# Performance work log

Hardware: AMD Instinct MI355X
Metric: run time of the kernel (lower is better)

Reference implementation:

```python
import jax, jax.numpy as jnp
import numpy as np

B, DH, P, V, NP, K = 8, 1024, 64, 50257, 256, 8
SKEW = P * (P - 1) // 2


def setup_inputs() -> dict:
    key = jax.random.key(0)
    ks = jax.random.split(key, 24)
    f = jax.random.normal
    h_t = f(ks[0], (B, DH), jnp.float32)
    R = f(ks[1], (B, P, P), jnp.float32)
    A_t = 0.05 * (R - jnp.swapaxes(R, -1, -2))  # skew-symmetric
    B_t = f(ks[2], (B, NP, P), jnp.float32)
    E = f(ks[3], (V, P), jnp.float32)
    e_mask = f(ks[4], (B, P), jnp.float32)
    M = f(ks[5], (B, P, P), jnp.float32)
    G_tilde = jnp.eye(P) + 0.01 * jnp.einsum('bij,bkj->bik', M, M)  # SPD metric
    z0 = f(ks[6], (B, P), jnp.float32)
    s = lambda k_, sh: f(k_, sh, jnp.float32) * 0.02
    params = dict(
        WQ_w=s(ks[7], (DH, P)), WQ_b=jnp.zeros((P,)),
        WK_w=s(ks[8], (P, P)), WK_b=jnp.zeros((P,)),
        WV_w=s(ks[9], (P, P)), WV_b=jnp.zeros((P,)),
        WC_w=s(ks[10], (P, P)), WC_b=jnp.zeros((P,)),
        WO_w=s(ks[11], (DH, V)),
        WG_w=s(ks[12], (P, P)), WG_b=jnp.zeros((P,)),
        wgamma_w=s(ks[13], (DH + P + SKEW, 1)), wgamma_b=jnp.zeros((1,)),
        wmu_w=s(ks[14], (DH + P + 2, 1)), wmu_b=jnp.zeros((1,)),
        gdown_w=s(ks[15], (SKEW, P)),
        Sigma_inv=jnp.ones((P,)) * 0.1,
        hlie_w=s(ks[16], (DH, P)), hlie_b=jnp.zeros((P,)),
    )
    return dict(h_t=h_t, A_t=A_t, B_t=B_t, E=E, e_mask=e_mask,
                G_tilde=G_tilde, z0=z0, **params)


def _sq_riem(x, Y, G):
    # x: (B,p), Y: (B,n,p), G: (B,p,p) -> (B,n)
    d = Y - x[:, None, :]
    return jnp.einsum('bnp,bpq,bnq->bn', d, G, d)


def reference(h_t, A_t, B_t, E, e_mask, G_tilde, z0,
              WQ_w, WQ_b, WK_w, WK_b, WV_w, WV_b, WC_w, WC_b, WO_w,
              WG_w, WG_b, wgamma_w, wgamma_b, wmu_w, wmu_b,
              gdown_w, Sigma_inv, hlie_w, hlie_b):
    p = A_t.shape[-1]
    scale = 1.0 / jnp.sqrt(jnp.asarray(p, h_t.dtype))
    I = jnp.eye(p, dtype=A_t.dtype)
    Q_t = jnp.linalg.solve(I - A_t, jnp.broadcast_to(I + A_t, A_t.shape))  # Cayley map (B,p,p)
    q_t = h_t @ WQ_w + WQ_b                      # (B,p)
    B_rot = jnp.einsum('bnp,bpq->bnq', B_t, Q_t)  # (B,n,p)
    K_t = B_rot @ WK_w + WK_b
    V_t = B_rot @ WV_w + WV_b
    h_lie = h_t @ hlie_w + hlie_b                 # (B,p)
    omega = -0.5 * _sq_riem(h_lie, B_rot, G_tilde)  # (B,n)
    scores = jnp.einsum('bp,bnp->bn', q_t, K_t) * scale + omega
    alpha = jax.nn.softmax(scores, axis=-1)
    c_t = jnp.einsum('bn,bnp->bp', alpha, V_t)
    iu0, iu1 = jnp.triu_indices(p, k=1)
    g_t = A_t[:, iu0, iu1]                        # (B, skew_dim)
    E_gen = E @ WG_w + WG_b                       # (V,p)
    g_proj = g_t @ gdown_w                        # (B,p)
    diff = E_gen[None, :, :] - g_proj[:, None, :]  # (B,V,p)
    kappa = -jnp.sum(diff * diff * Sigma_inv, axis=-1)  # (B,V)
    base_logits = h_t @ WO_w                      # (B,V)
    c_rot = jnp.einsum('bp,bpq->bq', c_t @ WC_w + WC_b, Q_t)
    group_logits = c_rot @ E.T * scale + kappa
    gamma = jax.nn.sigmoid(jnp.concatenate([h_t, c_t, g_t], -1) @ wgamma_w + wgamma_b)
    logits = base_logits + gamma * group_logits
    pi = jax.nn.softmax(logits, axis=-1)
    topv, topi = jax.lax.top_k(pi, K)
    topp = topv / jnp.sum(topv, -1, keepdims=True)
    E_g = E[topi]                                 # (B,k,p) gather
    E_G = jnp.einsum('bkp,bpq->bkq', E_g, Q_t)
    E_exp = jnp.einsum('bk,bkp->bp', topp, E_G)
    H = -jnp.sum(pi * jnp.log(pi + 1e-12), -1, keepdims=True)
    rho = _sq_riem(h_lie, E_exp[:, None, :], G_tilde)  # (B,1)
    mu = jax.nn.sigmoid(jnp.concatenate([h_t, c_t, H, rho], -1) @ wmu_w + wmu_b)
    m_next = mu * e_mask + (1.0 - mu) * E_exp
    outer = m_next[:, :, None] * e_mask[:, None, :]
    A_next = A_t + 0.1 * (outer - jnp.swapaxes(outer, 1, 2))
    return logits, m_next, A_next
```

## Files before the change

kernel.cpp:

```cpp
#include <hip/hip_runtime.h>
#include <math.h>

#define NV    50257
#define OUT_M 402056
#define OUT_A 402568
#define SCALE 0.125f

#define WS_Q      0
#define WS_HTR    32768
#define WS_S      40960
#define WS_TV     45056
#define WS_C0     45120
#define WS_HLIE   47144
#define WS_W1     47656
#define WS_GH     48176
#define WS_WMAT   48192
#define WS_SC     80960
#define WS_WB     83008
#define WS_CONSTB 83520
#define WS_GAMMA  83528
#define WS_CT     83536
#define WS_P6     84048
#define WS_PQT    86016
#define WS_PHL    94208
#define WS_PGH    102400
#define WS_PGP    102528
#define WS_PGG    118912

__global__ __launch_bounds__(256) void kA_prep(
    const float* __restrict__ h_t, const float* __restrict__ A_t,
    const float* __restrict__ WG_w, const float* __restrict__ WG_b,
    const float* __restrict__ Sigma_inv,
    const float* __restrict__ WQ_w, const float* __restrict__ wgamma_w,
    const float* __restrict__ hlie_w, const float* __restrict__ gdown_w,
    float* __restrict__ ws)
{
    __shared__ float Ash[64][65];
    __shared__ float Gsh[64][65];
    __shared__ float hsh[1024];
    __shared__ float piv[2][132];
    __shared__ float fr[2][64];
    __shared__ float dsh[64];

    const int tid = threadIdx.x;
    const int blk = blockIdx.x;

    if (blk < 8) {
        const int b  = blk;
        const int i  = tid & 63;
        const int cb = __builtin_amdgcn_readfirstlane(tid >> 6);

        for (int idx = tid; idx < 4096; idx += 256)
            Ash[idx >> 6][idx & 63] = A_t[b*4096 + idx];
        for (int k = tid; k < 1024; k += 256)
            ws[WS_HTR + k*8 + b] = h_t[b*1024 + k];
        __syncthreads();

        float w[32];
        if (cb < 2) {
            #pragma unroll
            for (int jj = 0; jj < 32; ++jj) {
                int j = cb*32 + jj;
                w[jj] = (i == j ? 1.0f : 0.0f) - Ash[i][j];
            }
        } else {
            #pragma unroll
            for (int jj = 0; jj < 32; ++jj) {
                int j = (cb - 2)*32 + jj;
                w[jj] = (i == j ? 1.0f : 0.0f) + Ash[i][j];
            }
        }
        __syncthreads();

        #pragma unroll
        for (int k = 0; k < 64; ++k) {
            const int kb  = k >> 5;
            const int sel = k & 1;
            if (cb == kb) fr[sel][i] = w[k & 31];
            if (i == k) {
                #pragma unroll
                for (int q4 = 0; q4 < 8; ++q4)
                    *(float4*)&piv[sel][cb*32 + q4*4] =
                        make_float4(w[q4*4], w[q4*4+1], w[q4*4+2], w[q4*4+3]);
            }
            __syncthreads();
            float pk = piv[sel][k];
            float f = (i == k) ? 0.0f : (fr[sel][i] / pk);
            #pragma unroll
            for (int jj = 0; jj < 32; ++jj)
                w[jj] -= f * piv[sel][cb*32 + jj];
        }

        if (cb == (i >> 5)) dsh[i] = w[i & 31];
        __syncthreads();
        if (cb >= 2) {
            float dinv = 1.0f / dsh[i];
            #pragma unroll
            for (int jj = 0; jj < 32; ++jj)
                Ash[i][(cb - 2)*32 + jj] = w[jj] * dinv;
        }
        __syncthreads();
        for (int idx = tid; idx < 4096; idx += 256)
            ws[WS_Q + b*4096 + idx] = Ash[idx >> 6][idx & 63];
        return;
    }

    if (blk == 8) {
        const int a   = tid & 63;
        const int cb8 = __builtin_amdgcn_readfirstlane(tid >> 6);
        float* sig = hsh;
        float* bg  = hsh + 64;
        if (tid < 64) { sig[tid] = Sigma_inv[tid]; bg[tid] = WG_b[tid]; }
        __syncthreads();
        for (int idx = tid; idx < 4096; idx += 256) {
            int r = idx >> 6, c = idx & 63;
            float wv = WG_w[idx];
            Gsh[r][c] = wv;
            Ash[r][c] = wv * sig[c];
        }
        __syncthreads();
        float t8[16];
        #pragma unroll
        for (int j = 0; j < 16; ++j) t8[j] = 0.0f;
        for (int p = 0; p < 64; ++p) {
            float wv = Ash[a][p];
            #pragma unroll
            for (int jj = 0; jj < 16; ++jj) t8[jj] = fmaf(wv, Gsh[cb8*16 + jj][p], t8[jj]);
        }
        #pragma unroll
        for (int jj = 0; jj < 16; ++jj)
            ws[WS_S + a*64 + cb8*16 + jj] = t8[jj];
        if (cb8 == 0) {
            float s = 0.0f;
            for (int p = 0; p < 64; ++p) s += Ash[a][p] * bg[p];
            ws[WS_TV + a] = 2.0f * s;
        }
        if (tid == 0) {
            float c0 = 0.0f;
            for (int p = 0; p < 64; ++p) c0 += sig[p] * bg[p] * bg[p];
            ws[WS_C0] = c0;
        }
        return;
    }

    if (blk < 25) {
        const int c = blk - 9;
        const int i = tid & 63;
        const int w = __builtin_amdgcn_readfirstlane(tid >> 6);
        for (int idx = tid; idx < 4096; idx += 256) {
            int r = idx >> 6, col = idx & 63;
            int krow = c*64 + r;
            Ash[r][col] = WQ_w[krow*64 + col];
            Gsh[r][col] = hlie_w[krow*64 + col];
        }
        for (int t = tid; t < 512; t += 256) {
            int b = t >> 6, kk = t & 63;
            hsh[b*64 + kk] = h_t[b*1024 + c*64 + kk];
        }
        if (tid < 64) dsh[tid] = wgamma_w[c*64 + tid];
        __syncthreads();
        const int b0 = 2*w, b1 = 2*w + 1;
        float q0 = 0, q1 = 0, l0 = 0, l1 = 0;
        #pragma unroll 8
        for (int kk = 0; kk < 64; ++kk) {
            float a = Ash[kk][i], g = Gsh[kk][i];
            float h0 = hsh[b0*64 + kk], h1 = hsh[b1*64 + kk];
            q0 = fmaf(h0, a, q0); q1 = fmaf(h1, a, q1);
            l0 = fmaf(h0, g, l0); l1 = fmaf(h1, g, l1);
        }
        ws[WS_PQT + (c*8 + b0)*64 + i] = q0;
        ws[WS_PQT + (c*8 + b1)*64 + i] = q1;
        ws[WS_PHL + (c*8 + b0)*64 + i] = l0;
        ws[WS_PHL + (c*8 + b1)*64 + i] = l1;
        float g0 = hsh[b0*64 + i] * dsh[i];
        float g1 = hsh[b1*64 + i] * dsh[i];
        #pragma unroll
        for (int off = 32; off > 0; off >>= 1) {
            g0 += __shfl_xor(g0, off);
            g1 += __shfl_xor(g1, off);
        }
        if (i == 0) {
            ws[WS_PGH + c*8 + b0] = g0;
            ws[WS_PGH + c*8 + b1] = g1;
        }
        return;
    }

    {
        const int c = blk - 25;
        const int i = tid & 63;
        const int w = __builtin_amdgcn_readfirstlane(tid >> 6);
        for (int idx = tid; idx < 4032; idx += 256) {
            int r = idx >> 6, col = idx & 63;
            Ash[r][col] = gdown_w[(c*63 + r)*64 + col];
        }
        for (int t = tid; t < 504; t += 256) {
            int b = t / 63, sl = t % 63;
            int s = c*63 + sl;
            int i2 = 0, f = 0;
            while (f + (63 - i2) <= s) { f += 63 - i2; ++i2; }
            int j2 = i2 + 1 + (s - f);
            hsh[b*63 + sl] = A_t[b*4096 + i2*64 + j2];
        }
        if (tid < 63) dsh[tid] = wgamma_w[1088 + c*63 + tid];
        __syncthreads();
        const int b0 = 2*w, b1 = 2*w + 1;
        float a0 = 0, a1 = 0;
        #pragma unroll 4
        for (int sl = 0; sl < 63; ++sl) {
            float gd = Ash[sl][i];
            a0 = fmaf(hsh[b0*63 + sl], gd, a0);
            a1 = fmaf(hsh[b1*63 + sl], gd, a1);
        }
        ws[WS_PGP + (c*8 + b0)*64 + i] = a0;
        ws[WS_PGP + (c*8 + b1)*64 + i] = a1;
        float g0 = (i < 63) ? hsh[b0*63 + i] * dsh[i] : 0.0f;
        float g1 = (i < 63) ? hsh[b1*63 + i] * dsh[i] : 0.0f;
        #pragma unroll
        for (int off = 32; off > 0; off >>= 1) {
            g0 += __shfl_xor(g0, off);
            g1 += __shfl_xor(g1, off);
        }
        if (i == 0) {
            ws[WS_PGG + c*8 + b0] = g0;
            ws[WS_PGG + c*8 + b1] = g1;
        }
    }
}

__global__ __launch_bounds__(256) void kB_chain(
    const float* __restrict__ G_t,
    const float* __restrict__ WQ_b, const float* __restrict__ WK_w,
    const float* __restrict__ hlie_b,
    float* __restrict__ ws)
{
    __shared__ float Qsh[64][65], Gsh[64][65];
    __shared__ float part[4][64], partb[4][64];
    __shared__ float qt[64], hl[64], qkv[64], v0[64];
    __shared__ float red16[16];

    const int b = blockIdx.x, tid = threadIdx.x;
    const int i = tid & 63;
    const int cb = __builtin_amdgcn_readfirstlane(tid >> 6);
    const int col0 = cb * 16;

    for (int idx = tid; idx < 4096; idx += 256) {
        int r = idx >> 6, c = idx & 63;
        Qsh[r][c] = ws[WS_Q + b*4096 + idx];
        Gsh[r][c] = G_t[b*4096 + idx];
    }
    {
        float aq = 0, ah = 0;
        #pragma unroll
        for (int cc = 0; cc < 4; ++cc) {
            int c = cb*4 + cc;
            aq += ws[WS_PQT + (c*8 + b)*64 + i];
            ah += ws[WS_PHL + (c*8 + b)*64 + i];
        }
        part[cb][i] = aq; partb[cb][i] = ah;
    }
    if (tid < 16) red16[tid] = ws[WS_PGH + tid*8 + b];
    __syncthreads();
    if (tid < 64) {
        qt[tid] = part[0][tid]+part[1][tid]+part[2][tid]+part[3][tid] + WQ_b[tid];
        hl[tid] = partb[0][tid]+partb[1][tid]+partb[2][tid]+partb[3][tid] + hlie_b[tid];
    }
    if (tid == 0) {
        float s = 0;
        #pragma unroll
        for (int j = 0; j < 16; ++j) s += red16[j];
        ws[WS_GH + b] = s;
    }
    __syncthreads();
    {
        float acc = 0;
        #pragma unroll
        for (int jj = 0; jj < 16; ++jj)
            acc = fmaf(WK_w[i*64 + col0 + jj], qt[col0 + jj], acc);
        part[cb][i] = acc;
    }
    __syncthreads();
    if (tid < 64) qkv[tid] = part[0][tid]+part[1][tid]+part[2][tid]+part[3][tid];
    __syncthreads();
    {
        float acc = 0;
        #pragma unroll
        for (int jj = 0; jj < 16; ++jj)
            acc = fmaf(Gsh[i][col0 + jj], hl[col0 + jj], acc);
        part[cb][i] = acc;
    }
    __syncthreads();
    if (tid < 64)
        v0[tid] = SCALE*qkv[tid] + part[0][tid]+part[1][tid]+part[2][tid]+part[3][tid];
    __syncthreads();
    {
        float acc = 0;
        #pragma unroll
        for (int jj = 0; jj < 16; ++jj)
            acc = fmaf(Qsh[i][col0 + jj], v0[col0 + jj], acc);
        part[cb][i] = acc;
    }
    __syncthreads();
    if (tid < 64) {
        ws[WS_W1 + b*64 + tid]   = part[0][tid]+part[1][tid]+part[2][tid]+part[3][tid];
        ws[WS_HLIE + b*64 + tid] = hl[tid];
    }
    float tt[16];
    #pragma unroll
    for (int j = 0; j < 16; ++j) tt[j] = 0;
    for (int r = 0; r < 64; ++r) {
        float qv = Qsh[i][r];
        #pragma unroll
        for (int j = 0; j < 16; ++j) tt[j] = fmaf(qv, Gsh[r][col0 + j], tt[j]);
    }
    __syncthreads();
    #pragma unroll
    for (int j = 0; j < 16; ++j) Gsh[i][col0 + j] = tt[j];
    __syncthreads();
    float w2r[16];
    #pragma unroll
    for (int j = 0; j < 16; ++j) w2r[j] = 0;
    for (int q = 0; q < 64; ++q) {
        float tv = Gsh[i][q];
        #pragma unroll
        for (int j = 0; j < 16; ++j) w2r[j] = fmaf(tv, Qsh[col0 + j][q], w2r[j]);
    }
    #pragma unroll
    for (int j = 0; j < 16; ++j)
        ws[WS_WMAT + b*4096 + (col0 + j)*64 + i] = w2r[j];
}

__global__ __launch_bounds__(256) void kC_scores(
    const float* __restrict__ B_t, float* __restrict__ ws)
{
    __shared__ float Bsh[64][65];
    __shared__ float Wsh[64][64];
    __shared__ float w1sh[64];
    __shared__ float part[4][64];
    const int b = blockIdx.x >> 2, q4 = blockIdx.x & 3;
    const int tid = threadIdx.x, lane = tid & 63;
    const int gu = __builtin_amdgcn_readfirstlane(tid >> 6);
    const int col0 = gu * 16;
    for (int idx = tid; idx < 4096; idx += 256) {
        int r = idx >> 6, c = idx & 63;
        Bsh[r][c] = B_t[b*16384 + (q4*64 + r)*64 + c];
        Wsh[r][c] = ws[WS_WMAT + b*4096 + idx];
    }
    if (tid < 64) w1sh[tid] = ws[WS_W1 + b*64 + tid];
    __syncthreads();
    float t[16];
    #pragma unroll
    for (int j = 0; j < 16; ++j) t[j] = 0;
    for (int p = 0; p < 64; ++p) {
        float bv = Bsh[lane][p];
        #pragma unroll
        for (int j = 0; j < 16; ++j) t[j] = fmaf(bv, Wsh[p][col0 + j], t[j]);
    }
    float ps = 0;
    #pragma unroll
    for (int j = 0; j < 16; ++j) ps += (w1sh[col0+j] - 0.5f*t[j]) * Bsh[lane][col0+j];
    part[gu][lane] = ps;
    __syncthreads();
    if (tid < 64)
        ws[WS_SC + b*256 + q4*64 + tid] =
            part[0][tid]+part[1][tid]+part[2][tid]+part[3][tid];
}

__global__ __launch_bounds__(256) void kD_mid(
    const float* __restrict__ B_t,
    const float* __restrict__ WV_w, const float* __restrict__ WV_b,
    const float* __restrict__ WC_w, const float* __restrict__ WC_b,
    const float* __restrict__ WG_w, const float* __restrict__ WG_b,
    const float* __restrict__ wgamma_w, const float* __restrict__ wgamma_b,
    const float* __restrict__ Sigma_inv,
    float* __restrict__ ws)
{
    __shared__ float alpha[256], rr[256];
    __shared__ float part[4][64];
    __shared__ float cBr[64], cB[64], ct[64], cw[64], crot[64], gp[64], uv[64];
    __shared__ float red32[32];
    const int b = blockIdx.x, tid = threadIdx.x, lane = tid & 63;
    const int gu = __builtin_amdgcn_readfirstlane(tid >> 6);
    const int col0 = gu * 16;
    const float* Qb = ws + WS_Q + b*4096;

    float sv = ws[WS_SC + b*256 + tid];
    rr[tid] = sv;
    if (tid < 32) red32[tid] = ws[WS_PGG + tid*8 + b];
    __syncthreads();
    for (int off = 128; off > 0; off >>= 1) { if (tid < off) rr[tid] = fmaxf(rr[tid], rr[tid+off]); __syncthreads(); }
    float smax = rr[0]; __syncthreads();
    float e = expf(sv - smax);
    rr[tid] = e; __syncthreads();
    for (int off = 128; off > 0; off >>= 1) { if (tid < off) rr[tid] += rr[tid+off]; __syncthreads(); }
    float den = rr[0]; __syncthreads();
    alpha[tid] = e / den;
    __syncthreads();
    {
        float acc = 0;
        for (int nn = 0; nn < 64; ++nn) {
            int n = gu*64 + nn;
            acc = fmaf(alpha[n], B_t[b*16384 + n*64 + lane], acc);
        }
        part[gu][lane] = acc;
    }
    __syncthreads();
    if (tid < 64) cBr[tid] = part[0][tid]+part[1][tid]+part[2][tid]+part[3][tid];
    __syncthreads();
    {
        float acc = 0;
        #pragma unroll
        for (int pp = 0; pp < 16; ++pp) { int p = col0+pp; acc = fmaf(cBr[p], Qb[p*64+lane], acc); }
        part[gu][lane] = acc;
    }
    __syncthreads();
    if (tid < 64) cB[tid] = part[0][tid]+part[1][tid]+part[2][tid]+part[3][tid];
    __syncthreads();
    {
        float acc = 0;
        #pragma unroll
        for (int pp = 0; pp < 16; ++pp) { int p = col0+pp; acc = fmaf(cB[p], WV_w[p*64+lane], acc); }
        part[gu][lane] = acc;
    }
    __syncthreads();
    if (tid < 64) {
        float v = part[0][tid]+part[1][tid]+part[2][tid]+part[3][tid] + WV_b[tid];
        ct[tid] = v; ws[WS_CT + b*64 + tid] = v;
    }
    __syncthreads();
    {
        float acc = 0;
        #pragma unroll
        for (int pp = 0; pp < 16; ++pp) { int p = col0+pp; acc = fmaf(ct[p], WC_w[p*64+lane], acc); }
        part[gu][lane] = acc;
    }
    __syncthreads();
    if (tid < 64) cw[tid] = part[0][tid]+part[1][tid]+part[2][tid]+part[3][tid] + WC_b[tid];
    __syncthreads();
    {
        float acc = 0;
        #pragma unroll
        for (int pp = 0; pp < 16; ++pp) { int p = col0+pp; acc = fmaf(cw[p], Qb[p*64+lane], acc); }
        part[gu][lane] = acc;
    }
    __syncthreads();
    if (tid < 64) crot[tid] = part[0][tid]+part[1][tid]+part[2][tid]+part[3][tid];
    __syncthreads();
    {
        float acc = 0;
        #pragma unroll
        for (int cc = 0; cc < 8; ++cc) {
            int c = gu*8 + cc;
            acc += ws[WS_PGP + (c*8 + b)*64 + lane];
        }
        part[gu][lane] = acc;
    }
    if (tid < 64) rr[64 + tid] = ct[tid] * wgamma_w[1024 + tid];
    __syncthreads();
    if (tid < 64) {
        float g = part[0][tid]+part[1][tid]+part[2][tid]+part[3][tid];
        gp[tid] = g; uv[tid] = 2.0f * Sigma_inv[tid] * g;
    }
    if (tid == 0) {
        float gc = 0;
        for (int j = 0; j < 64; ++j) gc += rr[64 + j];
        float ga = 0;
        for (int j = 0; j < 32; ++j) ga += red32[j];
        float z = ws[WS_GH + b] + gc + ga + wgamma_b[0];
        ws[WS_GAMMA + b] = 1.0f / (1.0f + expf(-z));
    }
    __syncthreads();
    {
        float acc = 0;
        #pragma unroll
        for (int pp = 0; pp < 16; ++pp) { int p = col0+pp; acc = fmaf(WG_w[lane*64+p], uv[p], acc); }
        part[gu][lane] = acc;
    }
    if (tid < 64) rr[tid] = WG_b[tid]*uv[tid] - gp[tid]*gp[tid]*Sigma_inv[tid];
    __syncthreads();
    if (tid < 64)
        ws[WS_WB + b*64 + tid] = SCALE*crot[tid]
            + part[0][tid]+part[1][tid]+part[2][tid]+part[3][tid];
    if (tid == 0) { float s = 0; for (int j = 0; j < 64; ++j) s += rr[j]; ws[WS_CONSTB + b] = s; }
}

#define KU 16
__global__ __launch_bounds__(256) void k5_logits(
    const float* __restrict__ E, const float* __restrict__ WO_w,
    const float* __restrict__ ws, float* __restrict__ out)
{
    __shared__ float smem[11600];
    const int tid = threadIdx.x;
    const int q   = tid >> 6;
    const int vt  = tid & 63;
    const int vb  = blockIdx.x * 64;
    const int v   = vb + vt;
    const bool vok = v < NV;
    const int vv = vok ? v : NV - 1;

    float* Esh  = smem;
    float* Ssh  = smem + 4224;
    float* tvsh = smem + 8448;
    float* wbsh = smem + 8512;
    float* gmsh = smem + 9024;
    float* cbsh = smem + 9032;
    float* svsh = smem + 9040;
    float* gdsh = smem + 9296;
    float* accsh= smem + 9872;
    float* hsh  = smem;

    for (int idx = tid; idx < 1024; idx += 256) {
        int r = idx >> 4, c4 = (idx & 15) * 4;
        int vr = vb + r; if (vr >= NV) vr = NV - 1;
        float4 e4 = *(const float4*)(E + (size_t)vr * 64 + c4);
        float* dst = Esh + r*66 + c4;
        dst[0] = e4.x; dst[1] = e4.y; dst[2] = e4.z; dst[3] = e4.w;
    }
    for (int idx = tid; idx < 4096; idx += 256) Ssh[idx] = ws[WS_S + idx];
    for (int idx = tid; idx < 512; idx += 256) wbsh[idx] = ws[WS_WB + idx];
    if (tid < 64) tvsh[tid] = ws[WS_TV + tid];
    if (tid < 8) { gmsh[tid] = ws[WS_GAMMA + tid]; cbsh[tid] = ws[WS_CONSTB + tid]; }
    __syncthreads();
    {
        const float* er = Esh + vt*66;
        float sv = (q == 0) ? ws[WS_C0] : 0.0f;
        {
            float t[16];
            #pragma unroll
            for (int j = 0; j < 16; ++j) t[j] = 0.0f;
            for (int p = 0; p < 64; ++p) {
                float ep = er[p];
                #pragma unroll
                for (int j = 0; j < 16; ++j)
                    t[j] = fmaf(ep, Ssh[p*64 + q*16 + j], t[j]);
            }
            #pragma unroll
            for (int j = 0; j < 16; ++j)
                sv += (t[j] + tvsh[q*16 + j]) * er[q*16 + j];
        }
        svsh[q*64 + vt] = sv;
        const float* w0 = wbsh + (2*q    )*64;
        const float* w1 = wbsh + (2*q + 1)*64;
        float g0 = 0, g1 = 0;
        #pragma unroll 8
        for (int p = 0; p < 64; ++p) {
            float ep = er[p];
            g0 = fmaf(ep, w0[p], g0); g1 = fmaf(ep, w1[p], g1);
        }
        gdsh[vt*9 + 2*q]     = g0;
        gdsh[vt*9 + 2*q + 1] = g1;
    }
    __syncthreads();
    for (int idx = tid; idx < 2048; idx += 256)
        *(float4*)(hsh + idx*4) = *(const float4*)(ws + WS_HTR + idx*4);
    __syncthreads();
    float acc[8];
    #pragma unroll
    for (int bb = 0; bb < 8; ++bb) acc[bb] = 0.0f;
    {
        const float* wo = WO_w + (size_t)(q * 256) * NV + vv;
        const float* hb = hsh + q*256*8;
        for (int k0 = 0; k0 < 256; k0 += KU) {
            float wr[KU];
            #pragma unroll
            for (int u = 0; u < KU; ++u) wr[u] = wo[(size_t)(k0 + u) * NV];
            #pragma unroll
            for (int u = 0; u < KU; ++u) {
                const float* hp = hb + (k0 + u)*8;
                #pragma unroll
                for (int bb = 0; bb < 8; ++bb) acc[bb] = fmaf(hp[bb], wr[u], acc[bb]);
            }
        }
    }
    if (q) {
        float* ar = accsh + (q-1)*576 + vt*9;
        #pragma unroll
        for (int bb = 0; bb < 8; ++bb) ar[bb] = acc[bb];
    }
    __syncthreads();
    if (q == 0 && vok) {
        float svt = svsh[vt] + svsh[64+vt] + svsh[128+vt] + svsh[192+vt];
        const float* gr = gdsh + vt*9;
        #pragma unroll
        for (int bb = 0; bb < 8; ++bb) {
            float a = acc[bb] + accsh[vt*9+bb] + accsh[576+vt*9+bb] + accsh[1152+vt*9+bb];
            float gl = gr[bb] + cbsh[bb] - svt;
            out[bb*NV + v] = fmaf(gmsh[bb], gl, a);
        }
    }
}

#define NQ 12565
__global__ __launch_bounds__(256) void k6a_scan(
    const float* __restrict__ outl, float* __restrict__ ws)
{
    __shared__ float mvw[4][8];
    __shared__ int   miw[4][8];
    __shared__ float t8v[8];
    __shared__ int   t8i[8];
    __shared__ float redv[4], sred[4];
    const int b = blockIdx.x >> 2, qq = blockIdx.x & 3;
    const int tid = threadIdx.x, lane = tid & 63, wvi = tid >> 6;
    const int v0 = qq * NQ;
    const int v1 = (v0 + NQ < NV) ? (v0 + NQ) : NV;
    const float* lg = outl + b*NV;

    float lv[8]; int li[8];
    #pragma unroll
    for (int u = 0; u < 8; ++u) { lv[u] = -INFINITY; li[u] = 0x7fffffff; }
    float mt = -INFINITY, s1 = 0.0f, s2 = 0.0f;
    for (int v = v0 + tid; v < v1; v += 256) {
        float x = lg[v];
        if (x > mt) {
            float r = expf(mt - x);
            s1 *= r; s2 *= r; mt = x;
        }
        float ee = expf(x - mt);
        s1 += ee; s2 += x * ee;
        if (x > lv[7]) {
            float cv = x; int ci = v;
            #pragma unroll
            for (int u = 0; u < 8; ++u) {
                if (cv > lv[u]) {
                    float tv = lv[u]; lv[u] = cv; cv = tv;
                    int   ti = li[u]; li[u] = ci; ci = ti;
                }
            }
        }
    }
    float wv8[8]; int wi8[8];
    #pragma unroll
    for (int it = 0; it < 8; ++it) {
        float bv = lv[0]; int bi = li[0];
        #pragma unroll
        for (int off = 32; off > 0; off >>= 1) {
            float ov = __shfl_xor(bv, off);
            int   oi = __shfl_xor(bi, off);
            if (ov > bv || (ov == bv && oi < bi)) { bv = ov; bi = oi; }
        }
        wv8[it] = bv; wi8[it] = bi;
        if (lv[0] == bv && li[0] == bi) {
            lv[0]=lv[1]; lv[1]=lv[2]; lv[2]=lv[3]; lv[3]=lv[4];
            lv[4]=lv[5]; lv[5]=lv[6]; lv[6]=lv[7]; lv[7]=-INFINITY;
            li[0]=li[1]; li[1]=li[2]; li[2]=li[3]; li[3]=li[4];
            li[4]=li[5]; li[5]=li[6]; li[6]=li[7]; li[7]=0x7fffffff;
        }
    }
    if (lane == 0) {
        #pragma unroll
        for (int u = 0; u < 8; ++u) { mvw[wvi][u] = wv8[u]; miw[wvi][u] = wi8[u]; }
    }
    __syncthreads();
    if (tid == 0) {
        int pA = 0, pB = 0, pC = 0, pD = 0;
        for (int it = 0; it < 8; ++it) {
            float vA = mvw[0][pA], vB = mvw[1][pB], vC = mvw[2][pC], vD = mvw[3][pD];
            int   iA = miw[0][pA], iB = miw[1][pB], iC = miw[2][pC], iD = miw[3][pD];
            float best = vA; int bi = iA; int w = 0;
            if (vB > best || (vB == best && iB < bi)) { best = vB; bi = iB; w = 1; }
            if (vC > best || (vC == best && iC < bi)) { best = vC; bi = iC; w = 2; }
            if (vD > best || (vD == best && iD < bi)) { best = vD; bi = iD; w = 3; }
            t8v[it] = best; t8i[it] = bi;
            if (w == 0) ++pA; else if (w == 1) ++pB; else if (w == 2) ++pC; else ++pD;
        }
    }
    __syncthreads();
    float Mp = t8v[0];
    {
        float r = expf(mt - Mp);
        s1 *= r; s2 *= r;
    }
    #pragma unroll
    for (int off = 32; off > 0; off >>= 1) {
        s1 += __shfl_xor(s1, off);
        s2 += __shfl_xor(s2, off);
    }
    if (lane == 0) { redv[wvi] = s1; sred[wvi] = s2; }
    __syncthreads();
    if (tid == 0) {
        int base = WS_P6 + (b*4 + qq)*20;
        #pragma unroll
        for (int u = 0; u < 8; ++u) { ws[base + u] = t8v[u]; ((int*)ws)[base + 8 + u] = t8i[u]; }
        ws[base + 16] = Mp;
        ws[base + 17] = redv[0]+redv[1]+redv[2]+redv[3];
        ws[base + 18] = sred[0]+sred[1]+sred[2]+sred[3];
    }
}

__global__ __launch_bounds__(256) void k6b_final(
    const float* __restrict__ h_t, const float* __restrict__ A_t,
    const float* __restrict__ E, const float* __restrict__ e_mask,
    const float* __restrict__ G_t,
    const float* __restrict__ wmu_w, const float* __restrict__ wmu_b,
    const float* __restrict__ ws, float* __restrict__ out)
{
    __shared__ float mv[32];
    __shared__ int   mi[32];
    __shared__ float t8v[8];
    __shared__ int   t8i[8];
    __shared__ float toppsh[8];
    __shared__ float redv[256];
    __shared__ float uvec[64], eexp[64], msh[64], emsh[64];
    __shared__ float scal[4];
    const int b = blockIdx.x, tid = threadIdx.x;

    if (tid < 32) {
        int base = WS_P6 + (b*4 + (tid >> 3))*20;
        mv[tid] = ws[base + (tid & 7)];
        mi[tid] = ((const int*)ws)[base + 8 + (tid & 7)];
    }
    __syncthreads();
    if (tid == 0) {
        unsigned used = 0;
        for (int it = 0; it < 8; ++it) {
            float best = -INFINITY; int bi = 0x7fffffff, bs = 0;
            for (int c = 0; c < 32; ++c) {
                if (used & (1u << c)) continue;
                float x = mv[c];
                if (x > best || (x == best && mi[c] < bi)) { best = x; bi = mi[c]; bs = c; }
            }
            used |= 1u << bs; t8v[it] = best; t8i[it] = bi;
        }
        float M = t8v[0];
        float s1 = 0, s2 = 0;
        for (int q = 0; q < 4; ++q) {
            int base = WS_P6 + (b*4 + q)*20;
            float sc_ = expf(ws[base + 16] - M);
            s1 += ws[base + 17] * sc_; s2 += ws[base + 18] * sc_;
        }
        scal[0] = M + logf(s1) - s2 / s1;
        float ts = 0, tv_[8];
        #pragma unroll
        for (int u = 0; u < 8; ++u) { tv_[u] = expf(t8v[u] - M); ts += tv_[u]; }
        #pragma unroll
        for (int u = 0; u < 8; ++u) toppsh[u] = tv_[u] / ts;
    }
    __syncthreads();
    if (tid < 64) {
        float u_ = 0;
        #pragma unroll
        for (int j = 0; j < 8; ++j) u_ += toppsh[j] * E[t8i[j]*64 + tid];
        uvec[tid] = u_;
    }
    __syncthreads();
    if (tid < 64) {
        const float* Qb = ws + WS_Q + b*4096;
        float a = 0;
        for (int p = 0; p < 64; ++p) a += uvec[p] * Qb[p*64 + tid];
        eexp[tid] = a;
    }
    __syncthreads();
    {
        const float* Gb = G_t + b*4096;
        const float* HL = ws + WS_HLIE + b*64;
        float a = 0;
        #pragma unroll 4
        for (int t2 = 0; t2 < 16; ++t2) {
            int idx = tid*16 + t2;
            int p = idx >> 6, q = idx & 63;
            a += (eexp[p] - HL[p]) * Gb[idx] * (eexp[q] - HL[q]);
        }
        redv[tid] = a;
    }
    __syncthreads();
    for (int off = 128; off > 0; off >>= 1) {
        if (tid < off) redv[tid] += redv[tid + off];
        __syncthreads();
    }
    if (tid == 0) scal[1] = redv[0];
    __syncthreads();
    float pm = 0;
    for (int k = tid; k < 1024; k += 256) pm += h_t[b*1024 + k] * wmu_w[k];
    if (tid < 64) pm += ws[WS_CT + b*64 + tid] * wmu_w[1024 + tid];
    redv[tid] = pm;
    __syncthreads();
    for (int off = 128; off > 0; off >>= 1) {
        if (tid < off) redv[tid] += redv[tid + off];
        __syncthreads();
    }
    if (tid == 0) {
        float z = redv[0] + scal[0]*wmu_w[1088] + scal[1]*wmu_w[1089] + wmu_b[0];
        scal[2] = 1.0f / (1.0f + expf(-z));
    }
    __syncthreads();
    if (tid < 64) {
        float mu = scal[2];
        float em = e_mask[b*64 + tid];
        float m = mu*em + (1.0f - mu)*eexp[tid];
        out[OUT_M + b*64 + tid] = m;
        msh[tid] = m; emsh[tid] = em;
    }
    __syncthreads();
    for (int idx = tid; idx < 4096; idx += 256) {
        int i = idx >> 6, j = idx & 63;
        out[OUT_A + b*4096 + idx] = A_t[b*4096 + idx]
            + 0.1f*(msh[i]*emsh[j] - msh[j]*emsh[i]);
    }
}

extern "C" void kernel_launch(void* const* d_in, const int* in_sizes, int n_in,
                              void* d_out, int out_size, void* d_ws, size_t ws_size,
                              hipStream_t stream)
{
    const float* h_t      = (const float*)d_in[0];
    const float* A_t      = (const float*)d_in[1];
    const float* B_t      = (const float*)d_in[2];
    const float* E        = (const float*)d_in[3];
    const float* e_mask   = (const float*)d_in[4];
    const float* G_t      = (const float*)d_in[5];
    const float* WQ_w     = (const float*)d_in[7];
    const float* WQ_b     = (const float*)d_in[8];
    const float* WK_w     = (const float*)d_in[9];
    const float* WV_w     = (const float*)d_in[11];
    const float* WV_b     = (const float*)d_in[12];
    const float* WC_w     = (const float*)d_in[13];
    const float* WC_b     = (const float*)d_in[14];
    const float* WO_w     = (const float*)d_in[15];
    const float* WG_w     = (const float*)d_in[16];
    const float* WG_b     = (const float*)d_in[17];
    const float* wgamma_w = (const float*)d_in[18];
    const float* wgamma_b = (const float*)d_in[19];
    const float* wmu_w    = (const float*)d_in[20];
    const float* wmu_b    = (const float*)d_in[21];
    const float* gdown_w  = (const float*)d_in[22];
    const float* Sigma_inv= (const float*)d_in[23];
    const float* hlie_w   = (const float*)d_in[24];
    const float* hlie_b   = (const float*)d_in[25];
    float* out = (float*)d_out;
    float* ws  = (float*)d_ws;

    kA_prep<<<57, 256, 0, stream>>>(h_t, A_t, WG_w, WG_b, Sigma_inv,
                                    WQ_w, wgamma_w, hlie_w, gdown_w, ws);
    kB_chain<<<8, 256, 0, stream>>>(G_t, WQ_b, WK_w, hlie_b, ws);
    kC_scores<<<32, 256, 0, stream>>>(B_t, ws);
    kD_mid<<<8, 256, 0, stream>>>(B_t, WV_w, WV_b, WC_w, WC_b, WG_w, WG_b,
                                  wgamma_w, wgamma_b, Sigma_inv, ws);
    k5_logits<<<786, 256, 0, stream>>>(E, WO_w, ws, out);
    k6a_scan<<<32, 256, 0, stream>>>(out, ws);
    k6b_final<<<8, 256, 0, stream>>>(h_t, A_t, E, e_mask, G_t, wmu_w, wmu_b, ws, out);
}
```

Before: 524.5 us.

## Fuse pipeline stages into a persistent cooperative megakernel with grid syncs

Replaces the chain of seven separate kernel launches with one cooperative persistent kernel that runs each stage as a device function, separated by grid-wide syncs. It keeps the original multi-launch path as a fallback. The logits stage also appears to be split into two passes (k5a/k5b) with per-block persistent setup and chunk loops. The goal is to remove launch gaps and small-kernel tail effects. In exchange it adds grid-sync overhead, a grid capped by occupancy, and a larger fixed shared-memory footprint per block.

```diff
diff --git a/kernel.cpp b/kernel.cpp
--- a/kernel.cpp
+++ b/kernel.cpp
@@ -1,5 +1,8 @@
 #include <hip/hip_runtime.h>
+#include <hip/hip_cooperative_groups.h>
 #include <math.h>
+
+namespace cg = cooperative_groups;
 
 #define NV    50257
 #define OUT_M 402056
@@ -26,367 +29,377 @@
 #define WS_PGH    102400
 #define WS_PGP    102528
 #define WS_PGG    118912
-
-__global__ __launch_bounds__(256) void kA_prep(
-    const float* __restrict__ h_t, const float* __restrict__ A_t,
-    const float* __restrict__ WG_w, const float* __restrict__ WG_b,
-    const float* __restrict__ Sigma_inv,
-    const float* __restrict__ WQ_w, const float* __restrict__ wgamma_w,
-    const float* __restrict__ hlie_w, const float* __restrict__ gdown_w,
-    float* __restrict__ ws)
-{
-    __shared__ float Ash[64][65];
-    __shared__ float Gsh[64][65];
-    __shared__ float hsh[1024];
-    __shared__ float piv[2][132];
-    __shared__ float fr[2][64];
-    __shared__ float dsh[64];
-
+#define WS_GL     131072
+
+#define SM_FLOATS 9760
+
+struct P {
+    const float *h_t, *A_t, *G_t, *B_t, *E, *e_mask;
+    const float *WG_w, *WG_b, *Sigma_inv, *WQ_w, *WQ_b, *WK_w;
+    const float *WV_w, *WV_b, *WC_w, *WC_b, *WO_w;
+    const float *wgamma_w, *wgamma_b, *wmu_w, *wmu_b, *gdown_w, *hlie_w, *hlie_b;
+    float *ws, *out;
+};
+
+
+__device__ void d_gj(float* sm, const P& p, int b)
+{
     const int tid = threadIdx.x;
-    const int blk = blockIdx.x;
-
-    if (blk < 8) {
-        const int b  = blk;
-        const int i  = tid & 63;
-        const int cb = __builtin_amdgcn_readfirstlane(tid >> 6);
-
-        for (int idx = tid; idx < 4096; idx += 256)
-            Ash[idx >> 6][idx & 63] = A_t[b*4096 + idx];
-        for (int k = tid; k < 1024; k += 256)
-            ws[WS_HTR + k*8 + b] = h_t[b*1024 + k];
+    const int i  = tid & 63;
+    const int cb = __builtin_amdgcn_readfirstlane(tid >> 6);
+    float* A   = sm;
+    float* piv = sm + 4160;
+    float* fr  = sm + 4424;
+    float* dsh = sm + 4552;
+    for (int idx = tid; idx < 4096; idx += 256)
+        A[(idx >> 6)*65 + (idx & 63)] = p.A_t[b*4096 + idx];
+    for (int k = tid; k < 1024; k += 256)
+        p.ws[WS_HTR + k*8 + b] = p.h_t[b*1024 + k];
+    __syncthreads();
+    float w[32];
+    if (cb < 2) {
+        #pragma unroll
+        for (int jj = 0; jj < 32; ++jj) {
+            int j = cb*32 + jj;
+            w[jj] = (i == j ? 1.0f : 0.0f) - A[i*65 + j];
+        }
+    } else {
+        #pragma unroll
+        for (int jj = 0; jj < 32; ++jj) {
+            int j = (cb - 2)*32 + jj;
+            w[jj] = (i == j ? 1.0f : 0.0f) + A[i*65 + j];
+        }
+    }
+    __syncthreads();
+    #pragma unroll
+    for (int k = 0; k < 64; ++k) {
+        const int kb = k >> 5, sel = k & 1;
+        if (cb == kb) fr[sel*64 + i] = w[k & 31];
+        if (i == k) {
+            #pragma unroll
+            for (int q4 = 0; q4 < 8; ++q4)
+                *(float4*)&piv[sel*132 + cb*32 + q4*4] =
+                    make_float4(w[q4*4], w[q4*4+1], w[q4*4+2], w[q4*4+3]);
+        }
         __syncthreads();
-
-        float w[32];
-        if (cb < 2) {
-            #pragma unroll
-            for (int jj = 0; jj < 32; ++jj) {
-                int j = cb*32 + jj;
-                w[jj] = (i == j ? 1.0f : 0.0f) - Ash[i][j];
-            }
-        } else {
-            #pragma unroll
-            for (int jj = 0; jj < 32; ++jj) {
-                int j = (cb - 2)*32 + jj;
-                w[jj] = (i == j ? 1.0f : 0.0f) + Ash[i][j];
-            }
-        }
-        __syncthreads();
-
-        #pragma unroll
-        for (int k = 0; k < 64; ++k) {
-            const int kb  = k >> 5;
-            const int sel = k & 1;
-            if (cb == kb) fr[sel][i] = w[k & 31];
-            if (i == k) {
-                #pragma unroll
-                for (int q4 = 0; q4 < 8; ++q4)
-                    *(float4*)&piv[sel][cb*32 + q4*4] =
-                        make_float4(w[q4*4], w[q4*4+1], w[q4*4+2], w[q4*4+3]);
-            }
-            __syncthreads();
-            float pk = piv[sel][k];
-            float f = (i == k) ? 0.0f : (fr[sel][i] / pk);
-            #pragma unroll
-            for (int jj = 0; jj < 32; ++jj)
-                w[jj] -= f * piv[sel][cb*32 + jj];
-        }
-
-        if (cb == (i >> 5)) dsh[i] = w[i & 31];
-        __syncthreads();
-        if (cb >= 2) {
-            float dinv = 1.0f / dsh[i];
-            #pragma unroll
-            for (int jj = 0; jj < 32; ++jj)
-                Ash[i][(cb - 2)*32 + jj] = w[jj] * dinv;
-        }
-        __syncthreads();
-        for (int idx = tid; idx < 4096; idx += 256)
-            ws[WS_Q + b*4096 + idx] = Ash[idx >> 6][idx & 63];
-        return;
-    }
-
-    if (blk == 8) {
-        const int a   = tid & 63;
-        const int cb8 = __builtin_amdgcn_readfirstlane(tid >> 6);
-        float* sig = hsh;
-        float* bg  = hsh + 64;
-        if (tid < 64) { sig[tid] = Sigma_inv[tid]; bg[tid] = WG_b[tid]; }
-        __syncthreads();
-        for (int idx = tid; idx < 4096; idx += 256) {
-            int r = idx >> 6, c = idx & 63;
-            float wv = WG_w[idx];
-            Gsh[r][c] = wv;
-            Ash[r][c] = wv * sig[c];
-        }
-        __syncthreads();
-        float t8[16];
-        #pragma unroll
-        for (int j = 0; j < 16; ++j) t8[j] = 0.0f;
-        for (int p = 0; p < 64; ++p) {
-            float wv = Ash[a][p];
-            #pragma unroll
-            for (int jj = 0; jj < 16; ++jj) t8[jj] = fmaf(wv, Gsh[cb8*16 + jj][p], t8[jj]);
-        }
+        float pk = piv[sel*132 + k];
+        float f = (i == k) ? 0.0f : (fr[sel*64 + i] / pk);
+        #pragma unroll
+        for (int jj = 0; jj < 32; ++jj)
+            w[jj] -= f * piv[sel*132 + cb*32 + jj];
+    }
+    if (cb == (i >> 5)) dsh[i] = w[i & 31];
+    __syncthreads();
+    if (cb >= 2) {
+        float dinv = 1.0f / dsh[i];
+        #pragma unroll
+        for (int jj = 0; jj < 32; ++jj)
+            A[i*65 + (cb - 2)*32 + jj] = w[jj] * dinv;
+    }
+    __syncthreads();
+    for (int idx = tid; idx < 4096; idx += 256)
+        p.ws[WS_Q + b*4096 + idx] = A[(idx >> 6)*65 + (idx & 63)];
+    __syncthreads();
+}
+
+__device__ void d_sphase(float* sm, const P& p)
+{
+    const int tid = threadIdx.x;
+    const int a   = tid & 63;
+    const int cb8 = __builtin_amdgcn_readfirstlane(tid >> 6);
+    float* sig = sm;
+    float* bg  = sm + 64;
+    float* Wsc = sm + 128;
+    float* Wr  = sm + 4288;
+    if (tid < 64) { sig[tid] = p.Sigma_inv[tid]; bg[tid] = p.WG_b[tid]; }
+    __syncthreads();
+    for (int idx = tid; idx < 4096; idx += 256) {
+        int r = idx >> 6, c = idx & 63;
+        float wv = p.WG_w[idx];
+        Wr[r*65 + c]  = wv;
+        Wsc[r*65 + c] = wv * sig[c];
+    }
+    __syncthreads();
+    float t8[16];
+    #pragma unroll
+    for (int j = 0; j < 16; ++j) t8[j] = 0.0f;
+    for (int pp = 0; pp < 64; ++pp) {
+        float wv = Wsc[a*65 + pp];
         #pragma unroll
         for (int jj = 0; jj < 16; ++jj)
-            ws[WS_S + a*64 + cb8*16 + jj] = t8[jj];
-        if (cb8 == 0) {
-            float s = 0.0f;
-            for (int p = 0; p < 64; ++p) s += Ash[a][p] * bg[p];
-            ws[WS_TV + a] = 2.0f * s;
-        }
-        if (tid == 0) {
-            float c0 = 0.0f;
-            for (int p = 0; p < 64; ++p) c0 += sig[p] * bg[p] * bg[p];
-            ws[WS_C0] = c0;
-        }
-        return;
-    }
-
-    if (blk < 25) {
-        const int c = blk - 9;
-        const int i = tid & 63;
-        const int w = __builtin_amdgcn_readfirstlane(tid >> 6);
-        for (int idx = tid; idx < 4096; idx += 256) {
-            int r = idx >> 6, col = idx & 63;
-            int krow = c*64 + r;
-            Ash[r][col] = WQ_w[krow*64 + col];
-            Gsh[r][col] = hlie_w[krow*64 + col];
-        }
-        for (int t = tid; t < 512; t += 256) {
-            int b = t >> 6, kk = t & 63;
-            hsh[b*64 + kk] = h_t[b*1024 + c*64 + kk];
-        }
-        if (tid < 64) dsh[tid] = wgamma_w[c*64 + tid];
-        __syncthreads();
-        const int b0 = 2*w, b1 = 2*w + 1;
-        float q0 = 0, q1 = 0, l0 = 0, l1 = 0;
-        #pragma unroll 8
-        for (int kk = 0; kk < 64; ++kk) {
-            float a = Ash[kk][i], g = Gsh[kk][i];
-            float h0 = hsh[b0*64 + kk], h1 = hsh[b1*64 + kk];
-            q0 = fmaf(h0, a, q0); q1 = fmaf(h1, a, q1);
-            l0 = fmaf(h0, g, l0); l1 = fmaf(h1, g, l1);
-        }
-        ws[WS_PQT + (c*8 + b0)*64 + i] = q0;
-        ws[WS_PQT + (c*8 + b1)*64 + i] = q1;
-        ws[WS_PHL + (c*8 + b0)*64 + i] = l0;
-        ws[WS_PHL + (c*8 + b1)*64 + i] = l1;
-        float g0 = hsh[b0*64 + i] * dsh[i];
-        float g1 = hsh[b1*64 + i] * dsh[i];
-        #pragma unroll
-        for (int off = 32; off > 0; off >>= 1) {
-            g0 += __shfl_xor(g0, off);
-            g1 += __shfl_xor(g1, off);
-        }
-        if (i == 0) {
-            ws[WS_PGH + c*8 + b0] = g0;
-            ws[WS_PGH + c*8 + b1] = g1;
-        }
-        return;
-    }
-
-    {
-        const int c = blk - 25;
-        const int i = tid & 63;
-        const int w = __builtin_amdgcn_readfirstlane(tid >> 6);
-        for (int idx = tid; idx < 4032; idx += 256) {
-            int r = idx >> 6, col = idx & 63;
-            Ash[r][col] = gdown_w[(c*63 + r)*64 + col];
-        }
-        for (int t = tid; t < 504; t += 256) {
-            int b = t / 63, sl = t % 63;
-            int s = c*63 + sl;
-            int i2 = 0, f = 0;
-            while (f + (63 - i2) <= s) { f += 63 - i2; ++i2; }
-            int j2 = i2 + 1 + (s - f);
-            hsh[b*63 + sl] = A_t[b*4096 + i2*64 + j2];
-        }
-        if (tid < 63) dsh[tid] = wgamma_w[1088 + c*63 + tid];
-        __syncthreads();
-        const int b0 = 2*w, b1 = 2*w + 1;
-        float a0 = 0, a1 = 0;
-        #pragma unroll 4
-        for (int sl = 0; sl < 63; ++sl) {
-            float gd = Ash[sl][i];
-            a0 = fmaf(hsh[b0*63 + sl], gd, a0);
-            a1 = fmaf(hsh[b1*63 + sl], gd, a1);
-        }
-        ws[WS_PGP + (c*8 + b0)*64 + i] = a0;
-        ws[WS_PGP + (c*8 + b1)*64 + i] = a1;
-        float g0 = (i < 63) ? hsh[b0*63 + i] * dsh[i] : 0.0f;
-        float g1 = (i < 63) ? hsh[b1*63 + i] * dsh[i] : 0.0f;
-        #pragma unroll
-        for (int off = 32; off > 0; off >>= 1) {
-            g0 += __shfl_xor(g0, off);
-            g1 += __shfl_xor(g1, off);
-        }
-        if (i == 0) {
-            ws[WS_PGG + c*8 + b0] = g0;
-            ws[WS_PGG + c*8 + b1] = g1;
-        }
-    }
-}
-
-__global__ __launch_bounds__(256) void kB_chain(
-    const float* __restrict__ G_t,
-    const float* __restrict__ WQ_b, const float* __restrict__ WK_w,
-    const float* __restrict__ hlie_b,
-    float* __restrict__ ws)
-{
-    __shared__ float Qsh[64][65], Gsh[64][65];
-    __shared__ float part[4][64], partb[4][64];
-    __shared__ float qt[64], hl[64], qkv[64], v0[64];
-    __shared__ float red16[16];
-
-    const int b = blockIdx.x, tid = threadIdx.x;
+            t8[jj] = fmaf(wv, Wr[(cb8*16 + jj)*65 + pp], t8[jj]);
+    }
+    #pragma unroll
+    for (int jj = 0; jj < 16; ++jj)
+        p.ws[WS_S + a*64 + cb8*16 + jj] = t8[jj];
+    if (cb8 == 0) {
+        float s = 0.0f;
+        for (int pp = 0; pp < 64; ++pp) s += Wsc[a*65 + pp] * bg[pp];
+        p.ws[WS_TV + a] = 2.0f * s;
+    }
+    if (tid == 0) {
+        float c0 = 0.0f;
+        for (int pp = 0; pp < 64; ++pp) c0 += sig[pp] * bg[pp] * bg[pp];
+        p.ws[WS_C0] = c0;
+    }
+    __syncthreads();
+}
+
+__device__ void d_hgemv(float* sm, const P& p, int c)
+{
+    const int tid = threadIdx.x;
+    const int i = tid & 63;
+    const int w = __builtin_amdgcn_readfirstlane(tid >> 6);
+    float* WQs = sm;
+    float* HLs = sm + 4160;
+    float* hh  = sm + 8320;
+    float* dd  = sm + 8832;
+    for (int idx = tid; idx < 4096; idx += 256) {
+        int r = idx >> 6, col = idx & 63;
+        int krow = c*64 + r;
+        WQs[r*65 + col] = p.WQ_w[krow*64 + col];
+        HLs[r*65 + col] = p.hlie_w[krow*64 + col];
+    }
+    for (int t = tid; t < 512; t += 256) {
+        int b = t >> 6, kk = t & 63;
+        hh[b*64 + kk] = p.h_t[b*1024 + c*64 + kk];
+    }
+    if (tid < 64) dd[tid] = p.wgamma_w[c*64 + tid];
+    __syncthreads();
+    const int b0 = 2*w, b1 = 2*w + 1;
+    float q0 = 0, q1 = 0, l0 = 0, l1 = 0;
+    #pragma unroll 8
+    for (int kk = 0; kk < 64; ++kk) {
+        float a = WQs[kk*65 + i], g = HLs[kk*65 + i];
+        float h0 = hh[b0*64 + kk], h1 = hh[b1*64 + kk];
+        q0 = fmaf(h0, a, q0); q1 = fmaf(h1, a, q1);
+        l0 = fmaf(h0, g, l0); l1 = fmaf(h1, g, l1);
+    }
+    p.ws[WS_PQT + (c*8 + b0)*64 + i] = q0;
+    p.ws[WS_PQT + (c*8 + b1)*64 + i] = q1;
+    p.ws[WS_PHL + (c*8 + b0)*64 + i] = l0;
+    p.ws[WS_PHL + (c*8 + b1)*64 + i] = l1;
+    float g0 = hh[b0*64 + i] * dd[i];
+    float g1 = hh[b1*64 + i] * dd[i];
+    #pragma unroll
+    for (int off = 32; off > 0; off >>= 1) {
+        g0 += __shfl_xor(g0, off);
+        g1 += __shfl_xor(g1, off);
+    }
+    if (i == 0) {
+        p.ws[WS_PGH + c*8 + b0] = g0;
+        p.ws[WS_PGH + c*8 + b1] = g1;
+    }
+    __syncthreads();
+}
+
+__device__ void d_gdown(float* sm, const P& p, int c)
+{
+    const int tid = threadIdx.x;
+    const int i = tid & 63;
+    const int w = __builtin_amdgcn_readfirstlane(tid >> 6);
+    float* GD = sm;
+    float* hh = sm + 4160;
+    float* dd = sm + 4672;
+    for (int idx = tid; idx < 4032; idx += 256) {
+        int r = idx >> 6, col = idx & 63;
+        GD[r*65 + col] = p.gdown_w[(c*63 + r)*64 + col];
+    }
+    for (int t = tid; t < 504; t += 256) {
+        int b = t / 63, sl = t % 63;
+        int s = c*63 + sl;
+        int i2 = 0, f = 0;
+        while (f + (63 - i2) <= s) { f += 63 - i2; ++i2; }
+        int j2 = i2 + 1 + (s - f);
+        hh[b*63 + sl] = p.A_t[b*4096 + i2*64 + j2];
+    }
+    if (tid < 63) dd[tid] = p.wgamma_w[1088 + c*63 + tid];
+    __syncthreads();
+    const int b0 = 2*w, b1 = 2*w + 1;
+    float a0 = 0, a1 = 0;
+    #pragma unroll 4
+    for (int sl = 0; sl < 63; ++sl) {
+        float gd = GD[sl*65 + i];
+        a0 = fmaf(hh[b0*63 + sl], gd, a0);
+        a1 = fmaf(hh[b1*63 + sl], gd, a1);
+    }
+    p.ws[WS_PGP + (c*8 + b0)*64 + i] = a0;
+    p.ws[WS_PGP + (c*8 + b1)*64 + i] = a1;
+    float g0 = (i < 63) ? hh[b0*63 + i] * dd[i] : 0.0f;
+    float g1 = (i < 63) ? hh[b1*63 + i] * dd[i] : 0.0f;
+    #pragma unroll
+    for (int off = 32; off > 0; off >>= 1) {
+        g0 += __shfl_xor(g0, off);
+        g1 += __shfl_xor(g1, off);
+    }
+    if (i == 0) {
+        p.ws[WS_PGG + c*8 + b0] = g0;
+        p.ws[WS_PGG + c*8 + b1] = g1;
+    }
+    __syncthreads();
+}
+
+__device__ void d_kB(float* sm, const P& p, int b)
+{
+    const int tid = threadIdx.x;
     const int i = tid & 63;
     const int cb = __builtin_amdgcn_readfirstlane(tid >> 6);
     const int col0 = cb * 16;
+    float* Q     = sm;
+    float* G     = sm + 4160;
+    float* part  = sm + 8320;
+    float* partb = sm + 8576;
+    float* qt    = sm + 8832;
+    float* hl    = sm + 8896;
+    float* qkv   = sm + 8960;
+    float* v0    = sm + 9024;
+    float* r16   = sm + 9088;
 
     for (int idx = tid; idx < 4096; idx += 256) {
         int r = idx >> 6, c = idx & 63;
-        Qsh[r][c] = ws[WS_Q + b*4096 + idx];
-        Gsh[r][c] = G_t[b*4096 + idx];
+        Q[r*65 + c] = p.ws[WS_Q + b*4096 + idx];
+        G[r*65 + c] = p.G_t[b*4096 + idx];
     }
     {
         float aq = 0, ah = 0;
         #pragma unroll
         for (int cc = 0; cc < 4; ++cc) {
             int c = cb*4 + cc;
-            aq += ws[WS_PQT + (c*8 + b)*64 + i];
-            ah += ws[WS_PHL + (c*8 + b)*64 + i];
-        }
-        part[cb][i] = aq; partb[cb][i] = ah;
-    }
-    if (tid < 16) red16[tid] = ws[WS_PGH + tid*8 + b];
+            aq += p.ws[WS_PQT + (c*8 + b)*64 + i];
+            ah += p.ws[WS_PHL + (c*8 + b)*64 + i];
+        }
+        part[cb*64 + i] = aq; partb[cb*64 + i] = ah;
+    }
+    if (tid < 16) r16[tid] = p.ws[WS_PGH + tid*8 + b];
     __syncthreads();
     if (tid < 64) {
-        qt[tid] = part[0][tid]+part[1][tid]+part[2][tid]+part[3][tid] + WQ_b[tid];
-        hl[tid] = partb[0][tid]+partb[1][tid]+partb[2][tid]+partb[3][tid] + hlie_b[tid];
+        qt[tid] = part[tid]+part[64+tid]+part[128+tid]+part[192+tid] + p.WQ_b[tid];
+        hl[tid] = partb[tid]+partb[64+tid]+partb[128+tid]+partb[192+tid] + p.hlie_b[tid];
     }
     if (tid == 0) {
         float s = 0;
         #pragma unroll
-        for (int j = 0; j < 16; ++j) s += red16[j];
-        ws[WS_GH + b] = s;
+        for (int j = 0; j < 16; ++j) s += r16[j];
+        p.ws[WS_GH + b] = s;
     }
     __syncthreads();
     {
         float acc = 0;
         #pragma unroll
         for (int jj = 0; jj < 16; ++jj)
-            acc = fmaf(WK_w[i*64 + col0 + jj], qt[col0 + jj], acc);
-        part[cb][i] = acc;
-    }
-    __syncthreads();
-    if (tid < 64) qkv[tid] = part[0][tid]+part[1][tid]+part[2][tid]+part[3][tid];
+            acc = fmaf(p.WK_w[i*64 + col0 + jj], qt[col0 + jj], acc);
+        part[cb*64 + i] = acc;
+    }
+    __syncthreads();
+    if (tid < 64) qkv[tid] = part[tid]+part[64+tid]+part[128+tid]+part[192+tid];
     __syncthreads();
     {
         float acc = 0;
         #pragma unroll
         for (int jj = 0; jj < 16; ++jj)
-            acc = fmaf(Gsh[i][col0 + jj], hl[col0 + jj], acc);
-        part[cb][i] = acc;
+            acc = fmaf(G[i*65 + col0 + jj], hl[col0 + jj], acc);
+        part[cb*64 + i] = acc;
     }
     __syncthreads();
     if (tid < 64)
-        v0[tid] = SCALE*qkv[tid] + part[0][tid]+part[1][tid]+part[2][tid]+part[3][tid];
+        v0[tid] = SCALE*qkv[tid] + part[tid]+part[64+tid]+part[128+tid]+part[192+tid];
     __syncthreads();
     {
         float acc = 0;
         #pragma unroll
         for (int jj = 0; jj < 16; ++jj)
-            acc = fmaf(Qsh[i][col0 + jj], v0[col0 + jj], acc);
-        part[cb][i] = acc;
+            acc = fmaf(Q[i*65 + col0 + jj], v0[col0 + jj], acc);
+        part[cb*64 + i] = acc;
     }
     __syncthreads();
     if (tid < 64) {
-        ws[WS_W1 + b*64 + tid]   = part[0][tid]+part[1][tid]+part[2][tid]+part[3][tid];
-        ws[WS_HLIE + b*64 + tid] = hl[tid];
+        p.ws[WS_W1 + b*64 + tid]   = part[tid]+part[64+tid]+part[128+tid]+part[192+tid];
+        p.ws[WS_HLIE + b*64 + tid] = hl[tid];
     }
     float tt[16];
     #pragma unroll
     for (int j = 0; j < 16; ++j) tt[j] = 0;
     for (int r = 0; r < 64; ++r) {
-        float qv = Qsh[i][r];
-        #pragma unroll
-        for (int j = 0; j < 16; ++j) tt[j] = fmaf(qv, Gsh[r][col0 + j], tt[j]);
-    }
-    __syncthreads();
-    #pragma unroll
-    for (int j = 0; j < 16; ++j) Gsh[i][col0 + j] = tt[j];
+        float qv = Q[i*65 + r];
+        #pragma unroll
+        for (int j = 0; j < 16; ++j) tt[j] = fmaf(qv, G[r*65 + col0 + j], tt[j]);
+    }
+    __syncthreads();
+    #pragma unroll
+    for (int j = 0; j < 16; ++j) G[i*65 + col0 + j] = tt[j];
     __syncthreads();
     float w2r[16];
     #pragma unroll
     for (int j = 0; j < 16; ++j) w2r[j] = 0;
     for (int q = 0; q < 64; ++q) {
-        float tv = Gsh[i][q];
-        #pragma unroll
-        for (int j = 0; j < 16; ++j) w2r[j] = fmaf(tv, Qsh[col0 + j][q], w2r[j]);
+        float tv = G[i*65 + q];
+        #pragma unroll
+        for (int j = 0; j < 16; ++j) w2r[j] = fmaf(tv, Q[(col0 + j)*65 + q], w2r[j]);
     }
     #pragma unroll
     for (int j = 0; j < 16; ++j)
-        ws[WS_WMAT + b*4096 + (col0 + j)*64 + i] = w2r[j];
-}
-
-__global__ __launch_bounds__(256) void kC_scores(
-    const float* __restrict__ B_t, float* __restrict__ ws)
-{
-    __shared__ float Bsh[64][65];
-    __shared__ float Wsh[64][64];
-    __shared__ float w1sh[64];
-    __shared__ float part[4][64];
-    const int b = blockIdx.x >> 2, q4 = blockIdx.x & 3;
+        p.ws[WS_WMAT + b*4096 + (col0 + j)*64 + i] = w2r[j];
+    __syncthreads();
+}
+
+__device__ void d_kC(float* sm, const P& p, int j)
+{
+    const int b = j >> 2, q4 = j & 3;
     const int tid = threadIdx.x, lane = tid & 63;
     const int gu = __builtin_amdgcn_readfirstlane(tid >> 6);
     const int col0 = gu * 16;
+    float* B    = sm;
+    float* W    = sm + 4160;
+    float* w1   = sm + 8256;
+    float* part = sm + 8320;
     for (int idx = tid; idx < 4096; idx += 256) {
         int r = idx >> 6, c = idx & 63;
-        Bsh[r][c] = B_t[b*16384 + (q4*64 + r)*64 + c];
-        Wsh[r][c] = ws[WS_WMAT + b*4096 + idx];
-    }
-    if (tid < 64) w1sh[tid] = ws[WS_W1 + b*64 + tid];
+        B[r*65 + c] = p.B_t[b*16384 + (q4*64 + r)*64 + c];
+        W[idx]      = p.ws[WS_WMAT + b*4096 + idx];
+    }
+    if (tid < 64) w1[tid] = p.ws[WS_W1 + b*64 + tid];
     __syncthreads();
     float t[16];
     #pragma unroll
-    for (int j = 0; j < 16; ++j) t[j] = 0;
-    for (int p = 0; p < 64; ++p) {
-        float bv = Bsh[lane][p];
-        #pragma unroll
-        for (int j = 0; j < 16; ++j) t[j] = fmaf(bv, Wsh[p][col0 + j], t[j]);
+    for (int jj = 0; jj < 16; ++jj) t[jj] = 0;
+    for (int pp = 0; pp < 64; ++pp) {
+        float bv = B[lane*65 + pp];
+        #pragma unroll
+        for (int jj = 0; jj < 16; ++jj) t[jj] = fmaf(bv, W[pp*64 + col0 + jj], t[jj]);
     }
     float ps = 0;
     #pragma unroll
-    for (int j = 0; j < 16; ++j) ps += (w1sh[col0+j] - 0.5f*t[j]) * Bsh[lane][col0+j];
-    part[gu][lane] = ps;
+    for (int jj = 0; jj < 16; ++jj)
+        ps += (w1[col0+jj] - 0.5f*t[jj]) * B[lane*65 + col0 + jj];
+    part[gu*64 + lane] = ps;
     __syncthreads();
     if (tid < 64)
-        ws[WS_SC + b*256 + q4*64 + tid] =
-            part[0][tid]+part[1][tid]+part[2][tid]+part[3][tid];
-}
-
-__global__ __launch_bounds__(256) void kD_mid(
-    const float* __restrict__ B_t,
-    const float* __restrict__ WV_w, const float* __restrict__ WV_b,
-    const float* __restrict__ WC_w, const float* __restrict__ WC_b,
-    const float* __restrict__ WG_w, const float* __restrict__ WG_b,
-    const float* __restrict__ wgamma_w, const float* __restrict__ wgamma_b,
-    const float* __restrict__ Sigma_inv,
-    float* __restrict__ ws)
-{
-    __shared__ float alpha[256], rr[256];
-    __shared__ float part[4][64];
-    __shared__ float cBr[64], cB[64], ct[64], cw[64], crot[64], gp[64], uv[64];
-    __shared__ float red32[32];
-    const int b = blockIdx.x, tid = threadIdx.x, lane = tid & 63;
+        p.ws[WS_SC + b*256 + q4*64 + tid] =
+            part[tid]+part[64+tid]+part[128+tid]+part[192+tid];
+    __syncthreads();
+}
+
+__device__ void d_kD(float* sm, const P& p, int b)
+{
+    const int tid = threadIdx.x, lane = tid & 63;
     const int gu = __builtin_amdgcn_readfirstlane(tid >> 6);
     const int col0 = gu * 16;
-    const float* Qb = ws + WS_Q + b*4096;
-
-    float sv = ws[WS_SC + b*256 + tid];
+    const float* Qb = p.ws + WS_Q + b*4096;
+    float* alpha = sm;
+    float* rr    = sm + 256;
+    float* part  = sm + 512;
+    float* cBr   = sm + 768;
+    float* cB    = sm + 832;
+    float* ct    = sm + 896;
+    float* cw    = sm + 960;
+    float* crot  = sm + 1024;
+    float* gp    = sm + 1088;
+    float* uv    = sm + 1152;
+    float* red32 = sm + 1216;
+
+    float sv = p.ws[WS_SC + b*256 + tid];
     rr[tid] = sv;
-    if (tid < 32) red32[tid] = ws[WS_PGG + tid*8 + b];
+    if (tid < 32) red32[tid] = p.ws[WS_PGG + tid*8 + b];
     __syncthreads();
     for (int off = 128; off > 0; off >>= 1) { if (tid < off) rr[tid] = fmaxf(rr[tid], rr[tid+off]); __syncthreads(); }
     float smax = rr[0]; __syncthreads();
@@ -400,210 +413,236 @@
         float acc = 0;
         for (int nn = 0; nn < 64; ++nn) {
             int n = gu*64 + nn;
-            acc = fmaf(alpha[n], B_t[b*16384 + n*64 + lane], acc);
-        }
-        part[gu][lane] = acc;
-    }
-    __syncthreads();
-    if (tid < 64) cBr[tid] = part[0][tid]+part[1][tid]+part[2][tid]+part[3][tid];
+            acc = fmaf(alpha[n], p.B_t[b*16384 + n*64 + lane], acc);
+        }
+        part[gu*64 + lane] = acc;
+    }
+    __syncthreads();
+    if (tid < 64) cBr[tid] = part[tid]+part[64+tid]+part[128+tid]+part[192+tid];
     __syncthreads();
     {
         float acc = 0;
         #pragma unroll
-        for (int pp = 0; pp < 16; ++pp) { int p = col0+pp; acc = fmaf(cBr[p], Qb[p*64+lane], acc); }
-        part[gu][lane] = acc;
-    }
-    __syncthreads();
-    if (tid < 64) cB[tid] = part[0][tid]+part[1][tid]+part[2][tid]+part[3][tid];
+        for (int pp = 0; pp < 16; ++pp) { int q = col0+pp; acc = fmaf(cBr[q], Qb[q*64+lane], acc); }
+        part[gu*64 + lane] = acc;
+    }
+    __syncthreads();
+    if (tid < 64) cB[tid] = part[tid]+part[64+tid]+part[128+tid]+part[192+tid];
     __syncthreads();
     {
         float acc = 0;
         #pragma unroll
-        for (int pp = 0; pp < 16; ++pp) { int p = col0+pp; acc = fmaf(cB[p], WV_w[p*64+lane], acc); }
-        part[gu][lane] = acc;
+        for (int pp = 0; pp < 16; ++pp) { int q = col0+pp; acc = fmaf(cB[q], p.WV_w[q*64+lane], acc); }
+        part[gu*64 + lane] = acc;
     }
     __syncthreads();
     if (tid < 64) {
-        float v = part[0][tid]+part[1][tid]+part[2][tid]+part[3][tid] + WV_b[tid];
-        ct[tid] = v; ws[WS_CT + b*64 + tid] = v;
+        float v = part[tid]+part[64+tid]+part[128+tid]+part[192+tid] + p.WV_b[tid];
+        ct[tid] = v; p.ws[WS_CT + b*64 + tid] = v;
     }
     __syncthreads();
     {
         float acc = 0;
         #pragma unroll
-        for (int pp = 0; pp < 16; ++pp) { int p = col0+pp; acc = fmaf(ct[p], WC_w[p*64+lane], acc); }
-        part[gu][lane] = acc;
-    }
-    __syncthreads();
-    if (tid < 64) cw[tid] = part[0][tid]+part[1][tid]+part[2][tid]+part[3][tid] + WC_b[tid];
+        for (int pp = 0; pp < 16; ++pp) { int q = col0+pp; acc = fmaf(ct[q], p.WC_w[q*64+lane], acc); }
+        part[gu*64 + lane] = acc;
+    }
+    __syncthreads();
+    if (tid < 64) cw[tid] = part[tid]+part[64+tid]+part[128+tid]+part[192+tid] + p.WC_b[tid];
     __syncthreads();
     {
         float acc = 0;
         #pragma unroll
-        for (int pp = 0; pp < 16; ++pp) { int p = col0+pp; acc = fmaf(cw[p], Qb[p*64+lane], acc); }
-        part[gu][lane] = acc;
-    }
-    __syncthreads();
-    if (tid < 64) crot[tid] = part[0][tid]+part[1][tid]+part[2][tid]+part[3][tid];
+        for (int pp = 0; pp < 16; ++pp) { int q = col0+pp; acc = fmaf(cw[q], Qb[q*64+lane], acc); }
+        part[gu*64 + lane] = acc;
+    }
+    __syncthreads();
+    if (tid < 64) crot[tid] = part[tid]+part[64+tid]+part[128+tid]+part[192+tid];
     __syncthreads();
     {
         float acc = 0;
         #pragma unroll
         for (int cc = 0; cc < 8; ++cc) {
             int c = gu*8 + cc;
-            acc += ws[WS_PGP + (c*8 + b)*64 + lane];
-        }
-        part[gu][lane] = acc;
-    }
-    if (tid < 64) rr[64 + tid] = ct[tid] * wgamma_w[1024 + tid];
+            acc += p.ws[WS_PGP + (c*8 + b)*64 + lane];
+        }
+        part[gu*64 + lane] = acc;
+    }
+    if (tid < 64) rr[64 + tid] = ct[tid] * p.wgamma_w[1024 + tid];
     __syncthreads();
     if (tid < 64) {
-        float g = part[0][tid]+part[1][tid]+part[2][tid]+part[3][tid];
-        gp[tid] = g; uv[tid] = 2.0f * Sigma_inv[tid] * g;
+        float g = part[tid]+part[64+tid]+part[128+tid]+part[192+tid];
+        gp[tid] = g; uv[tid] = 2.0f * p.Sigma_inv[tid] * g;
     }
     if (tid == 0) {
         float gc = 0;
         for (int j = 0; j < 64; ++j) gc += rr[64 + j];
         float ga = 0;
         for (int j = 0; j < 32; ++j) ga += red32[j];
-        float z = ws[WS_GH + b] + gc + ga + wgamma_b[0];
-        ws[WS_GAMMA + b] = 1.0f / (1.0f + expf(-z));
+        float z = p.ws[WS_GH + b] + gc + ga + p.wgamma_b[0];
+        p.ws[WS_GAMMA + b] = 1.0f / (1.0f + expf(-z));
     }
     __syncthreads();
     {
         float acc = 0;
         #pragma unroll
-        for (int pp = 0; pp < 16; ++pp) { int p = col0+pp; acc = fmaf(WG_w[lane*64+p], uv[p], acc); }
-        part[gu][lane] = acc;
-    }
-    if (tid < 64) rr[tid] = WG_b[tid]*uv[tid] - gp[tid]*gp[tid]*Sigma_inv[tid];
+        for (int pp = 0; pp < 16; ++pp) { int q = col0+pp; acc = fmaf(p.WG_w[lane*64+q], uv[q], acc); }
+        part[gu*64 + lane] = acc;
+    }
+    if (tid < 64) rr[tid] = p.WG_b[tid]*uv[tid] - gp[tid]*gp[tid]*p.Sigma_inv[tid];
     __syncthreads();
     if (tid < 64)
-        ws[WS_WB + b*64 + tid] = SCALE*crot[tid]
-            + part[0][tid]+part[1][tid]+part[2][tid]+part[3][tid];
-    if (tid == 0) { float s = 0; for (int j = 0; j < 64; ++j) s += rr[j]; ws[WS_CONSTB + b] = s; }
-}
-
-#define KU 16
-__global__ __launch_bounds__(256) void k5_logits(
-    const float* __restrict__ E, const float* __restrict__ WO_w,
-    const float* __restrict__ ws, float* __restrict__ out)
-{
-    __shared__ float smem[11600];
+        p.ws[WS_WB + b*64 + tid] = SCALE*crot[tid]
+            + part[tid]+part[64+tid]+part[128+tid]+part[192+tid];
+    if (tid == 0) { float s = 0; for (int j = 0; j < 64; ++j) s += rr[j]; p.ws[WS_CONSTB + b] = s; }
+    __syncthreads();
+}
+
+__device__ void d_k5a_persist(float* sm, const P& p)
+{
     const int tid = threadIdx.x;
-    const int q   = tid >> 6;
-    const int vt  = tid & 63;
-    const int vb  = blockIdx.x * 64;
-    const int v   = vb + vt;
+    for (int idx = tid; idx < 4096; idx += 256) sm[idx] = p.ws[WS_S + idx];
+    if (tid < 64) sm[4096 + tid] = p.ws[WS_TV + tid];
+    for (int idx = tid; idx < 512; idx += 256) sm[4160 + idx] = p.ws[WS_WB + idx];
+    if (tid < 8) {
+        sm[4672 + tid] = p.ws[WS_GAMMA + tid];
+        sm[4680 + tid] = p.ws[WS_CONSTB + tid];
+    }
+}
+
+__device__ void d_k5a_chunk(float* sm, const P& p, int c)
+{
+    const int tid = threadIdx.x;
+    const int vt = tid & 63;
+    const int q  = __builtin_amdgcn_readfirstlane(tid >> 6);
+    const int vb = c * 64;
+    const int v  = vb + vt;
     const bool vok = v < NV;
-    const int vv = vok ? v : NV - 1;
-
-    float* Esh  = smem;
-    float* Ssh  = smem + 4224;
-    float* tvsh = smem + 8448;
-    float* wbsh = smem + 8512;
-    float* gmsh = smem + 9024;
-    float* cbsh = smem + 9032;
-    float* svsh = smem + 9040;
-    float* gdsh = smem + 9296;
-    float* accsh= smem + 9872;
-    float* hsh  = smem;
+    float* S  = sm;
+    float* tv = sm + 4096;
+    float* wb = sm + 4160;
+    float* gm = sm + 4672;
+    float* cbs= sm + 4680;
+    float* E  = sm + 4688;
+    float* svs= sm + 8912;
+    float* gds= sm + 9168;
 
     for (int idx = tid; idx < 1024; idx += 256) {
         int r = idx >> 4, c4 = (idx & 15) * 4;
         int vr = vb + r; if (vr >= NV) vr = NV - 1;
-        float4 e4 = *(const float4*)(E + (size_t)vr * 64 + c4);
-        float* dst = Esh + r*66 + c4;
+        float4 e4 = *(const float4*)(p.E + (size_t)vr * 64 + c4);
+        float* dst = E + r*66 + c4;
         dst[0] = e4.x; dst[1] = e4.y; dst[2] = e4.z; dst[3] = e4.w;
     }
-    for (int idx = tid; idx < 4096; idx += 256) Ssh[idx] = ws[WS_S + idx];
-    for (int idx = tid; idx < 512; idx += 256) wbsh[idx] = ws[WS_WB + idx];
-    if (tid < 64) tvsh[tid] = ws[WS_TV + tid];
-    if (tid < 8) { gmsh[tid] = ws[WS_GAMMA + tid]; cbsh[tid] = ws[WS_CONSTB + tid]; }
-    __syncthreads();
-    {
-        const float* er = Esh + vt*66;
-        float sv = (q == 0) ? ws[WS_C0] : 0.0f;
-        {
-            float t[16];
-            #pragma unroll
-            for (int j = 0; j < 16; ++j) t[j] = 0.0f;
-            for (int p = 0; p < 64; ++p) {
-                float ep = er[p];
-                #pragma unroll
-                for (int j = 0; j < 16; ++j)
-                    t[j] = fmaf(ep, Ssh[p*64 + q*16 + j], t[j]);
-            }
+    __syncthreads();
+    {
+        const float* er = E + vt*66;
+        float sv = (q == 0) ? p.ws[WS_C0] : 0.0f;
+        float t[16];
+        #pragma unroll
+        for (int j = 0; j < 16; ++j) t[j] = 0.0f;
+        for (int pp = 0; pp < 64; ++pp) {
+            float ep = er[pp];
             #pragma unroll
             for (int j = 0; j < 16; ++j)
-                sv += (t[j] + tvsh[q*16 + j]) * er[q*16 + j];
-        }
-        svsh[q*64 + vt] = sv;
-        const float* w0 = wbsh + (2*q    )*64;
-        const float* w1 = wbsh + (2*q + 1)*64;
+                t[j] = fmaf(ep, S[pp*64 + q*16 + j], t[j]);
+        }
+        #pragma unroll
+        for (int j = 0; j < 16; ++j)
+            sv += (t[j] + tv[q*16 + j]) * er[q*16 + j];
+        svs[q*64 + vt] = sv;
+        const float* w0 = wb + (2*q    )*64;
+        const float* w1 = wb + (2*q + 1)*64;
         float g0 = 0, g1 = 0;
         #pragma unroll 8
-        for (int p = 0; p < 64; ++p) {
-            float ep = er[p];
-            g0 = fmaf(ep, w0[p], g0); g1 = fmaf(ep, w1[p], g1);
-        }
-        gdsh[vt*9 + 2*q]     = g0;
-        gdsh[vt*9 + 2*q + 1] = g1;
-    }
-    __syncthreads();
+        for (int pp = 0; pp < 64; ++pp) {
+            float ep = er[pp];
+            g0 = fmaf(ep, w0[pp], g0); g1 = fmaf(ep, w1[pp], g1);
+        }
+        gds[vt*9 + 2*q]     = g0;
+        gds[vt*9 + 2*q + 1] = g1;
+    }
+    __syncthreads();
+    if (q == 0 && vok) {
+        float svt = svs[vt] + svs[64+vt] + svs[128+vt] + svs[192+vt];
+        const float* gr = gds + vt*9;
+        #pragma unroll
+        for (int bb = 0; bb < 8; ++bb)
+            p.ws[WS_GL + bb*NV + v] = gm[bb] * (gr[bb] + cbs[bb] - svt);
+    }
+}
+
+__device__ void d_k5b_persist(float* sm, const P& p)
+{
+    const int tid = threadIdx.x;
     for (int idx = tid; idx < 2048; idx += 256)
-        *(float4*)(hsh + idx*4) = *(const float4*)(ws + WS_HTR + idx*4);
-    __syncthreads();
+        *(float4*)(sm + idx*4) = *(const float4*)(p.ws + WS_HTR + idx*4);
+}
+
+__device__ void d_k5b_chunk(float* sm, const P& p, int c)
+{
+    const int tid = threadIdx.x;
+    const int vt = tid & 63;
+    const int kg = __builtin_amdgcn_readfirstlane(tid >> 6);
+    const int vb = c * 64;
+    const int v  = vb + vt;
+    const bool vok = v < NV;
+    const int vv = vok ? v : NV - 1;
+    float* h   = sm;
+    float* red = sm + 8192;
+
     float acc[8];
     #pragma unroll
     for (int bb = 0; bb < 8; ++bb) acc[bb] = 0.0f;
     {
-        const float* wo = WO_w + (size_t)(q * 256) * NV + vv;
-        const float* hb = hsh + q*256*8;
-        for (int k0 = 0; k0 < 256; k0 += KU) {
-            float wr[KU];
+        const float* wo = p.WO_w + (size_t)(kg * 256) * NV + vv;
+        const float* hb = h + kg*256*8;
+        for (int k0 = 0; k0 < 256; k0 += 8) {
+            float wr[8];
             #pragma unroll
-            for (int u = 0; u < KU; ++u) wr[u] = wo[(size_t)(k0 + u) * NV];
+            for (int u = 0; u < 8; ++u) wr[u] = wo[(size_t)(k0 + u) * NV];
             #pragma unroll
-            for (int u = 0; u < KU; ++u) {
+            for (int u = 0; u < 8; ++u) {
                 const float* hp = hb + (k0 + u)*8;
                 #pragma unroll
                 for (int bb = 0; bb < 8; ++bb) acc[bb] = fmaf(hp[bb], wr[u], acc[bb]);
             }
         }
     }
-    if (q) {
-        float* ar = accsh + (q-1)*576 + vt*9;
-        #pragma unroll
-        for (int bb = 0; bb < 8; ++bb) ar[bb] = acc[bb];
-    }
-    __syncthreads();
-    if (q == 0 && vok) {
-        float svt = svsh[vt] + svsh[64+vt] + svsh[128+vt] + svsh[192+vt];
-        const float* gr = gdsh + vt*9;
-        #pragma unroll
-        for (int bb = 0; bb < 8; ++bb) {
-            float a = acc[bb] + accsh[vt*9+bb] + accsh[576+vt*9+bb] + accsh[1152+vt*9+bb];
-            float gl = gr[bb] + cbsh[bb] - svt;
-            out[bb*NV + v] = fmaf(gmsh[bb], gl, a);
-        }
+    float gl[8];
+    if (kg == 0) {
+        #pragma unroll
+        for (int bb = 0; bb < 8; ++bb) gl[bb] = p.ws[WS_GL + bb*NV + vv];
+    }
+    __syncthreads();
+    if (kg >= 1) {
+        float* r = red + (kg - 1)*512 + vt*8;
+        #pragma unroll
+        for (int bb = 0; bb < 8; ++bb) r[bb] = acc[bb];
+    }
+    __syncthreads();
+    if (kg == 0 && vok) {
+        #pragma unroll
+        for (int bb = 0; bb < 8; ++bb)
+            p.out[bb*NV + v] = acc[bb] + red[vt*8+bb] + red[512+vt*8+bb]
+                             + red[1024+vt*8+bb] + gl[bb];
     }
 }
 
 #define NQ 12565
-__global__ __launch_bounds__(256) void k6a_scan(
-    const float* __restrict__ outl, float* __restrict__ ws)
-{
-    __shared__ float mvw[4][8];
-    __shared__ int   miw[4][8];
-    __shared__ float t8v[8];
-    __shared__ int   t8i[8];
-    __shared__ float redv[4], sred[4];
-    const int b = blockIdx.x >> 2, qq = blockIdx.x & 3;
+__device__ void d_k6a(float* sm, const P& p, int j)
+{
+    const int b = j >> 2, qq = j & 3;
     const int tid = threadIdx.x, lane = tid & 63, wvi = tid >> 6;
     const int v0 = qq * NQ;
     const int v1 = (v0 + NQ < NV) ? (v0 + NQ) : NV;
-    const float* lg = outl + b*NV;
+    const float* lg = p.out + b*NV;
+    float* mvw = sm;
+    int*   miw = (int*)(sm + 32);
+    float* t8v = sm + 64;
+    int*   t8i = (int*)(sm + 72);
+    float* redv= sm + 80;
+    float* sred= sm + 84;
 
     float lv[8]; int li[8];
     #pragma unroll
@@ -622,7 +661,7 @@
             #pragma unroll
             for (int u = 0; u < 8; ++u) {
                 if (cv > lv[u]) {
-                    float tv = lv[u]; lv[u] = cv; cv = tv;
+                    float tv2 = lv[u]; lv[u] = cv; cv = tv2;
                     int   ti = li[u]; li[u] = ci; ci = ti;
                 }
             }
@@ -648,14 +687,14 @@
     }
     if (lane == 0) {
         #pragma unroll
-        for (int u = 0; u < 8; ++u) { mvw[wvi][u] = wv8[u]; miw[wvi][u] = wi8[u]; }
+        for (int u = 0; u < 8; ++u) { mvw[wvi*8 + u] = wv8[u]; miw[wvi*8 + u] = wi8[u]; }
     }
     __syncthreads();
     if (tid == 0) {
         int pA = 0, pB = 0, pC = 0, pD = 0;
         for (int it = 0; it < 8; ++it) {
-            float vA = mvw[0][pA], vB = mvw[1][pB], vC = mvw[2][pC], vD = mvw[3][pD];
-            int   iA = miw[0][pA], iB = miw[1][pB], iC = miw[2][pC], iD = miw[3][pD];
+            float vA = mvw[0*8+pA], vB = mvw[1*8+pB], vC = mvw[2*8+pC], vD = mvw[3*8+pD];
+            int   iA = miw[0*8+pA], iB = miw[1*8+pB], iC = miw[2*8+pC], iD = miw[3*8+pD];
             float best = vA; int bi = iA; int w = 0;
             if (vB > best || (vB == best && iB < bi)) { best = vB; bi = iB; w = 1; }
             if (vC > best || (vC == best && iC < bi)) { best = vC; bi = iC; w = 2; }
@@ -680,34 +719,33 @@
     if (tid == 0) {
         int base = WS_P6 + (b*4 + qq)*20;
         #pragma unroll
-        for (int u = 0; u < 8; ++u) { ws[base + u] = t8v[u]; ((int*)ws)[base + 8 + u] = t8i[u]; }
-        ws[base + 16] = Mp;
-        ws[base + 17] = redv[0]+redv[1]+redv[2]+redv[3];
-        ws[base + 18] = sred[0]+sred[1]+sred[2]+sred[3];
-    }
-}
-
-__global__ __launch_bounds__(256) void k6b_final(
-    const float* __restrict__ h_t, const float* __restrict__ A_t,
-    const float* __restrict__ E, const float* __restrict__ e_mask,
-    const float* __restrict__ G_t,
-    const float* __restrict__ wmu_w, const float* __restrict__ wmu_b,
-    const float* __restrict__ ws, float* __restrict__ out)
-{
-    __shared__ float mv[32];
-    __shared__ int   mi[32];
-    __shared__ float t8v[8];
-    __shared__ int   t8i[8];
-    __shared__ float toppsh[8];
-    __shared__ float redv[256];
-    __shared__ float uvec[64], eexp[64], msh[64], emsh[64];
-    __shared__ float scal[4];
-    const int b = blockIdx.x, tid = threadIdx.x;
+        for (int u = 0; u < 8; ++u) { p.ws[base + u] = t8v[u]; ((int*)p.ws)[base + 8 + u] = t8i[u]; }
+        p.ws[base + 16] = Mp;
+        p.ws[base + 17] = redv[0]+redv[1]+redv[2]+redv[3];
+        p.ws[base + 18] = sred[0]+sred[1]+sred[2]+sred[3];
+    }
+    __syncthreads();
+}
+
+__device__ void d_k6b(float* sm, const P& p, int b)
+{
+    const int tid = threadIdx.x;
+    float* mv   = sm;
+    int*   mi   = (int*)(sm + 32);
+    float* t8v  = sm + 64;
+    int*   t8i  = (int*)(sm + 72);
+    float* topp = sm + 80;
+    float* scal = sm + 88;
+    float* uvec = sm + 96;
+    float* eexp = sm + 160;
+    float* msh  = sm + 224;
+    float* emsh = sm + 288;
+    float* redv = sm + 352;
 
     if (tid < 32) {
         int base = WS_P6 + (b*4 + (tid >> 3))*20;
-        mv[tid] = ws[base + (tid & 7)];
-        mi[tid] = ((const int*)ws)[base + 8 + (tid & 7)];
+        mv[tid] = p.ws[base + (tid & 7)];
+        mi[tid] = ((const int*)p.ws)[base + 8 + (tid & 7)];
     }
     __syncthreads();
     if (tid == 0) {
@@ -725,40 +763,40 @@
         float s1 = 0, s2 = 0;
         for (int q = 0; q < 4; ++q) {
             int base = WS_P6 + (b*4 + q)*20;
-            float sc_ = expf(ws[base + 16] - M);
-            s1 += ws[base + 17] * sc_; s2 += ws[base + 18] * sc_;
+            float sc_ = expf(p.ws[base + 16] - M);
+            s1 += p.ws[base + 17] * sc_; s2 += p.ws[base + 18] * sc_;
         }
         scal[0] = M + logf(s1) - s2 / s1;
         float ts = 0, tv_[8];
         #pragma unroll
         for (int u = 0; u < 8; ++u) { tv_[u] = expf(t8v[u] - M); ts += tv_[u]; }
         #pragma unroll
-        for (int u = 0; u < 8; ++u) toppsh[u] = tv_[u] / ts;
+        for (int u = 0; u < 8; ++u) topp[u] = tv_[u] / ts;
     }
     __syncthreads();
     if (tid < 64) {
         float u_ = 0;
         #pragma unroll
-        for (int j = 0; j < 8; ++j) u_ += toppsh[j] * E[t8i[j]*64 + tid];
+        for (int j = 0; j < 8; ++j) u_ += topp[j] * p.E[t8i[j]*64 + tid];
         uvec[tid] = u_;
     }
     __syncthreads();
     if (tid < 64) {
-        const float* Qb = ws + WS_Q + b*4096;
+        const float* Qb = p.ws + WS_Q + b*4096;
         float a = 0;
-        for (int p = 0; p < 64; ++p) a += uvec[p] * Qb[p*64 + tid];
+        for (int pp = 0; pp < 64; ++pp) a += uvec[pp] * Qb[pp*64 + tid];
         eexp[tid] = a;
     }
     __syncthreads();
     {
-        const float* Gb = G_t + b*4096;
-        const float* HL = ws + WS_HLIE + b*64;
+        const float* Gb = p.G_t + b*4096;
+        const float* HL = p.ws + WS_HLIE + b*64;
         float a = 0;
         #pragma unroll 4
         for (int t2 = 0; t2 < 16; ++t2) {
             int idx = tid*16 + t2;
-            int p = idx >> 6, q = idx & 63;
-            a += (eexp[p] - HL[p]) * Gb[idx] * (eexp[q] - HL[q]);
+            int pp = idx >> 6, q = idx & 63;
+            a += (eexp[pp] - HL[pp]) * Gb[idx] * (eexp[q] - HL[q]);
         }
         redv[tid] = a;
     }
@@ -770,8 +808,8 @@
     if (tid == 0) scal[1] = redv[0];
     __syncthreads();
     float pm = 0;
-    for (int k = tid; k < 1024; k += 256) pm += h_t[b*1024 + k] * wmu_w[k];
-    if (tid < 64) pm += ws[WS_CT + b*64 + tid] * wmu_w[1024 + tid];
+    for (int k = tid; k < 1024; k += 256) pm += p.h_t[b*1024 + k] * p.wmu_w[k];
+    if (tid < 64) pm += p.ws[WS_CT + b*64 + tid] * p.wmu_w[1024 + tid];
     redv[tid] = pm;
     __syncthreads();
     for (int off = 128; off > 0; off >>= 1) {
@@ -779,63 +817,155 @@
         __syncthreads();
     }
     if (tid == 0) {
-        float z = redv[0] + scal[0]*wmu_w[1088] + scal[1]*wmu_w[1089] + wmu_b[0];
+        float z = redv[0] + scal[0]*p.wmu_w[1088] + scal[1]*p.wmu_w[1089] + p.wmu_b[0];
         scal[2] = 1.0f / (1.0f + expf(-z));
     }
     __syncthreads();
     if (tid < 64) {
         float mu = scal[2];
-        float em = e_mask[b*64 + tid];
+        float em = p.e_mask[b*64 + tid];
         float m = mu*em + (1.0f - mu)*eexp[tid];
-        out[OUT_M + b*64 + tid] = m;
+        p.out[OUT_M + b*64 + tid] = m;
         msh[tid] = m; emsh[tid] = em;
     }
     __syncthreads();
     for (int idx = tid; idx < 4096; idx += 256) {
         int i = idx >> 6, j = idx & 63;
-        out[OUT_A + b*4096 + idx] = A_t[b*4096 + idx]
+        p.out[OUT_A + b*4096 + idx] = p.A_t[b*4096 + idx]
             + 0.1f*(msh[i]*emsh[j] - msh[j]*emsh[i]);
     }
+    __syncthreads();
+}
+
+__global__ __launch_bounds__(256) void mega(P p)
+{
+    __shared__ float sm[SM_FLOATS];
+    cg::grid_group g = cg::this_grid();
+    const int blk = blockIdx.x, gdim = gridDim.x;
+
+    for (int j = blk; j < 57; j += gdim) {
+        if (j < 8)       d_gj(sm, p, j);
+        else if (j == 8) d_sphase(sm, p);
+        else if (j < 25) d_hgemv(sm, p, j - 9);
+        else             d_gdown(sm, p, j - 25);
+    }
+    g.sync();
+    for (int j = blk; j < 8;  j += gdim) d_kB(sm, p, j);
+    g.sync();
+    for (int j = blk; j < 32; j += gdim) d_kC(sm, p, j);
+    g.sync();
+    for (int j = blk; j < 8;  j += gdim) d_kD(sm, p, j);
+    g.sync();
+    d_k5a_persist(sm, p); __syncthreads();
+    for (int c = blk; c < 786; c += gdim) d_k5a_chunk(sm, p, c);
+    g.sync();
+    d_k5b_persist(sm, p); __syncthreads();
+    for (int c = blk; c < 786; c += gdim) d_k5b_chunk(sm, p, c);
+    g.sync();
+    for (int j = blk; j < 32; j += gdim) d_k6a(sm, p, j);
+    g.sync();
+    for (int j = blk; j < 8;  j += gdim) d_k6b(sm, p, j);
+}
+
+__global__ __launch_bounds__(256) void kA_prep(P p)
+{
+    __shared__ float sm[SM_FLOATS];
+    int j = blockIdx.x;
+    if (j < 8)       d_gj(sm, p, j);
+    else if (j == 8) d_sphase(sm, p);
+    else if (j < 25) d_hgemv(sm, p, j - 9);
+    else             d_gdown(sm, p, j - 25);
+}
+__global__ __launch_bounds__(256) void kB_k(P p)
+{
+    __shared__ float sm[SM_FLOATS];
+    d_kB(sm, p, blockIdx.x);
+}
+__global__ __launch_bounds__(256) void kC_k(P p)
+{
+    __shared__ float sm[SM_FLOATS];
+    d_kC(sm, p, blockIdx.x);
+}
+__global__ __launch_bounds__(256) void kD_k(P p)
+{
+    __shared__ float sm[SM_FLOATS];
+    d_kD(sm, p, blockIdx.x);
+}
+__global__ __launch_bounds__(256) void k5a_k(P p)
+{
+    __shared__ float sm[SM_FLOATS];
+    d_k5a_persist(sm, p); __syncthreads();
+    for (int c = blockIdx.x; c < 786; c += gridDim.x) d_k5a_chunk(sm, p, c);
+}
+__global__ __launch_bounds__(256) void k5b_k(P p)
+{
+    __shared__ float sm[SM_FLOATS];
+    d_k5b_persist(sm, p); __syncthreads();
+    for (int c = blockIdx.x; c < 786; c += gridDim.x) d_k5b_chunk(sm, p, c);
+}
+__global__ __launch_bounds__(256) void k6a_k(P p)
+{
+    __shared__ float sm[SM_FLOATS];
+    d_k6a(sm, p, blockIdx.x);
+}
+__global__ __launch_bounds__(256) void k6b_k(P p)
+{
+    __shared__ float sm[SM_FLOATS];
+    d_k6b(sm, p, blockIdx.x);
 }
 
 extern "C" void kernel_launch(void* const* d_in, const int* in_sizes, int n_in,
                               void* d_out, int out_size, void* d_ws, size_t ws_size,
                               hipStream_t stream)
 {
-    const float* h_t      = (const float*)d_in[0];
-    const float* A_t      = (const float*)d_in[1];
-    const float* B_t      = (const float*)d_in[2];
-    const float* E        = (const float*)d_in[3];
-    const float* e_mask   = (const float*)d_in[4];
-    const float* G_t      = (const float*)d_in[5];
-    const float* WQ_w     = (const float*)d_in[7];
-    const float* WQ_b     = (const float*)d_in[8];
-    const float* WK_w     = (const float*)d_in[9];
-    const float* WV_w     = (const float*)d_in[11];
-    const float* WV_b     = (const float*)d_in[12];
-    const float* WC_w     = (const float*)d_in[13];
-    const float* WC_b     = (const float*)d_in[14];
-    const float* WO_w     = (const float*)d_in[15];
-    const float* WG_w     = (const float*)d_in[16];
-    const float* WG_b     = (const float*)d_in[17];
-    const float* wgamma_w = (const float*)d_in[18];
-    const float* wgamma_b = (const float*)d_in[19];
-    const float* wmu_w    = (const float*)d_in[20];
-    const float* wmu_b    = (const float*)d_in[21];
-    const float* gdown_w  = (const float*)d_in[22];
-    const float* Sigma_inv= (const float*)d_in[23];
-    const float* hlie_w   = (const float*)d_in[24];
-    const float* hlie_b   = (const float*)d_in[25];
-    float* out = (float*)d_out;
-    float* ws  = (float*)d_ws;
-
-    kA_prep<<<57, 256, 0, stream>>>(h_t, A_t, WG_w, WG_b, Sigma_inv,
-                                    WQ_w, wgamma_w, hlie_w, gdown_w, ws);
-    kB_chain<<<8, 256, 0, stream>>>(G_t, WQ_b, WK_w, hlie_b, ws);
-    kC_scores<<<32, 256, 0, stream>>>(B_t, ws);
-    kD_mid<<<8, 256, 0, stream>>>(B_t, WV_w, WV_b, WC_w, WC_b, WG_w, WG_b,
-                                  wgamma_w, wgamma_b, Sigma_inv, ws);
-    k5_logits<<<786, 256, 0, stream>>>(E, WO_w, ws, out);
-    k6a_scan<<<32, 256, 0, stream>>>(out, ws);
-    k6b_final<<<8, 256, 0, stream>>>(h_t, A_t, E, e_mask, G_t, wmu_w, wmu_b, ws, out);
-}
+    P p;
+    p.h_t      = (const float*)d_in[0];
+    p.A_t      = (const float*)d_in[1];
+    p.B_t      = (const float*)d_in[2];
+    p.E        = (const float*)d_in[3];
+    p.e_mask   = (const float*)d_in[4];
+    p.G_t      = (const float*)d_in[5];
+    p.WQ_w     = (const float*)d_in[7];
+    p.WQ_b     = (const float*)d_in[8];
+    p.WK_w     = (const float*)d_in[9];
+    p.WV_w     = (const float*)d_in[11];
+    p.WV_b     = (const float*)d_in[12];
+    p.WC_w     = (const float*)d_in[13];
+    p.WC_b     = (const float*)d_in[14];
+    p.WO_w     = (const float*)d_in[15];
+    p.WG_w     = (const float*)d_in[16];
+    p.WG_b     = (const float*)d_in[17];
+    p.wgamma_w = (const float*)d_in[18];
+    p.wgamma_b = (const float*)d_in[19];
+    p.wmu_w    = (const float*)d_in[20];
+    p.wmu_b    = (const float*)d_in[21];
+    p.gdown_w  = (const float*)d_in[22];
+    p.Sigma_inv= (const float*)d_in[23];
+    p.hlie_w   = (const float*)d_in[24];
+    p.hlie_b   = (const float*)d_in[25];
+    p.ws  = (float*)d_ws;
+    p.out = (float*)d_out;
+
+    int maxB = 0;
+    hipError_t e = hipOccupancyMaxActiveBlocksPerMultiprocessor(
+        &maxB, (const void*)mega, 256, 0);
+    bool done = false;
+    if (e == hipSuccess && maxB >= 1) {
+        int nblk = maxB * 256;
+        if (nblk > 1024) nblk = 1024;
+        void* args[] = { (void*)&p };
+        e = hipLaunchCooperativeKernel((const void*)mega, dim3(nblk),
+                                       dim3(256, 1, 1), args, 0, stream);
+        if (e == hipSuccess) done = true;
+    }
+    if (!done) {
+        kA_prep<<<57,  256, 0, stream>>>(p);
+        kB_k  <<<8,   256, 0, stream>>>(p);
+        kC_k  <<<32,  256, 0, stream>>>(p);
+        kD_k  <<<8,   256, 0, stream>>>(p);
+        k5a_k <<<786, 256, 0, stream>>>(p);
+        k5b_k <<<786, 256, 0, stream>>>(p);
+        k6a_k <<<32,  256, 0, stream>>>(p);
+        k6b_k <<<8,   256, 0, stream>>>(p);
+    }
+}
```

Result: slower. 754.4 us (+43.8%).
